# Kernel optimization log

Hardware: AMD Instinct MI355X
Metric: run time of the kernel (lower is better)

The kernel has to match this reference:

```python
import jax, jax.numpy as jnp
import numpy as np

EPS = 1e-6

def _ln(x, g, b):
    m = jnp.mean(x, -1, keepdims=True)
    v = jnp.mean((x - m) ** 2, -1, keepdims=True)
    return (x - m) * jax.lax.rsqrt(v + 1e-5) * g + b

def _mha(qin, kin, vin, wq, bq, wk, bk, wv, bv, wo, bo, nh=8):
    B, T, D = qin.shape
    S = kin.shape[1]
    dh = D // nh
    q = (qin @ wq + bq).reshape(B, T, nh, dh)
    k = (kin @ wk + bk).reshape(B, S, nh, dh)
    v = (vin @ wv + bv).reshape(B, S, nh, dh)
    a = jax.nn.softmax(jnp.einsum('bthd,bshd->bhts', q, k) / np.float32(np.sqrt(dh)), -1)
    o = jnp.einsum('bhts,bshd->bthd', a, v).reshape(B, T, D)
    return o @ wo + bo

def _sinu_pe(pos, num_feats=128, temperature=20.0):
    # pos: [..., 2] (x, y); returns [..., 2*num_feats] ordered (y-feats, x-feats)
    dim_t = temperature ** ((2 * (jnp.arange(num_feats) // 2)) / num_feats)
    e = pos[..., None] * (2 * np.pi) / dim_t  # [..., 2, F]
    e = jnp.stack([jnp.sin(e[..., 0::2]), jnp.cos(e[..., 1::2])], -1).reshape(e.shape)
    return jnp.concatenate([e[..., 1, :], e[..., 0, :]], -1)

def _spatial36(b1, b2, sizes):
    # b1, b2: [B, Q, 4]; sizes: [B, 2] = (h, w). UPT-style 18 feats + log -> 36.
    h = sizes[:, 0:1]; w = sizes[:, 1:2]
    c1x = (b1[..., 0] + b1[..., 2]) / 2; c1y = (b1[..., 1] + b1[..., 3]) / 2
    c2x = (b2[..., 0] + b2[..., 2]) / 2; c2y = (b2[..., 1] + b2[..., 3]) / 2
    w1 = b1[..., 2] - b1[..., 0]; h1 = b1[..., 3] - b1[..., 1]
    w2 = b2[..., 2] - b2[..., 0]; h2 = b2[..., 3] - b2[..., 1]
    a1 = w1 * h1; a2 = w2 * h2
    dx = jnp.abs(c2x - c1x) / (w1 + EPS)
    dy = jnp.abs(c2y - c1y) / (h1 + EPS)
    ix = jnp.clip(jnp.minimum(b1[..., 2], b2[..., 2]) - jnp.maximum(b1[..., 0], b2[..., 0]), 0)
    iy = jnp.clip(jnp.minimum(b1[..., 3], b2[..., 3]) - jnp.maximum(b1[..., 1], b2[..., 1]), 0)
    inter = ix * iy
    iou = inter / (a1 + a2 - inter + EPS)
    f = jnp.stack([c1x / w, c1y / h, c2x / w, c2y / h, w1 / w, h1 / h, w2 / w, h2 / h,
                   a1 / (h * w), a2 / (h * w), a2 / (a1 + EPS), w1 / (h1 + EPS), w2 / (h2 + EPS), iou,
                   (c2x > c1x) * dx, (c2x < c1x) * dx, (c2y > c1y) * dy, (c2y < c1y) * dy], -1)
    return jnp.concatenate([f, jnp.log(f + EPS)], -1)

def _forward(boxes, embeds, image_sizes, pose, line, sw1, sb1, sw2, sb2, sw3, sb3, bw, bb, pw, pb, lw, lb, enc_pe_w, enc_pe_b, enc_qkv_w, enc_qkv_b, enc_out_w, enc_out_b, enc_ff1_w, enc_ff1_b, enc_ff2_w, enc_ff2_b, enc_ln1_g, enc_ln1_b, enc_ln2_g, enc_ln2_b, dec_q_w, dec_q_b, dec_kv_w, dec_kv_b, dec_out_w, dec_out_b, dec_ff1_w, dec_ff1_b, dec_ff2_w, dec_ff2_b, dec_ln1_g, dec_ln1_b, dec_ln2_g, dec_ln2_b, fc1_w, fc1_b, fc2_w, fc2_b, mln1_g, mln1_b, mln2_g, mln2_b, m1_w, m1_b, m2_w, m2_b, labels, nh):
    B, N, _ = boxes.shape
    # static human-object pairing (x != y) & (x < nh)
    xg, yg = np.meshgrid(np.arange(N), np.arange(N), indexing='ij')
    keep = (xg != yg) & (xg < nh)
    xk = jnp.asarray(xg[keep]); yk = jnp.asarray(yg[keep])  # [P]
    # line features: adaptive-avg-pool(1,1) + 1x1 conv == spatial mean + linear
    line_feat = jnp.mean(line, axis=(2, 3)) @ lw + lb  # [B, 256]
    # spatial head on all N*N ordered pairs, then gather kept pairs
    xa = jnp.asarray(xg.reshape(-1)); ya = jnp.asarray(yg.reshape(-1))
    f36 = _spatial36(boxes[:, xa], boxes[:, ya], image_sizes)  # [B, N*N, 36]
    s = jax.nn.relu(f36 @ sw1 + sb1)
    s = jax.nn.relu(s @ sw2 + sb2)
    s = jax.nn.relu(s @ sw3 + sb3)
    spa = s.reshape(B, N, N, -1)[:, xk, yk]  # [B, P, R]
    # box sinusoidal positional encodings (cat of centre-PE and wh-PE)
    whwh = image_sizes[:, jnp.array([1, 0, 1, 0])][:, None]  # [B,1,4]
    bxn = boxes / whwh
    ctr = (bxn[..., :2] + bxn[..., 2:]) / 2
    whb = bxn[..., 2:] - bxn[..., :2]
    box_pe = jnp.concatenate([_sinu_pe(ctr), _sinu_pe(whb)], -1)  # [B, N, 512]
    # 2-layer transformer encoder over instance tokens (pos added to q,k)
    posx = box_pe @ enc_pe_w + enc_pe_b
    x = embeds
    for i in range(enc_qkv_w.shape[0]):
        wq, wk_, wv = jnp.split(enc_qkv_w[i], 3, axis=1)
        bq, bk_, bv = jnp.split(enc_qkv_b[i], 3)
        qk = x + posx
        att = _mha(qk, qk, x, wq, bq, wk_, bk_, wv, bv, enc_out_w[i], enc_out_b[i])
        x = _ln(x + att, enc_ln1_g[i], enc_ln1_b[i])
        ff = jax.nn.relu(x @ enc_ff1_w[i] + enc_ff1_b[i]) @ enc_ff2_w[i] + enc_ff2_b[i]
        x = _ln(x + ff, enc_ln2_g[i], enc_ln2_b[i])
    # pair gather + human/object positional embeds (box PE projected + line feature)
    pe_h = box_pe[:, xk] @ bw + bb + line_feat[:, None, :]
    pe_o = box_pe[:, yk] @ bw + bb + line_feat[:, None, :]
    h = x[:, xk]; o = x[:, yk]  # [B, P, 256]
    pose_ctx = pose @ pw + pb  # [B, M, 256]
    # HO refine decoder: cross-attention from pair tokens to pose tokens
    for l in range(dec_q_w.shape[0]):
        wk_, wv = jnp.split(dec_kv_w[l], 2, axis=1)
        bk_, bv = jnp.split(dec_kv_b[l], 2)
        def _layer(feat, pe):
            att = _mha(feat + pe, pose_ctx, pose_ctx, dec_q_w[l], dec_q_b[l], wk_, bk_, wv, bv, dec_out_w[l], dec_out_b[l])
            feat = _ln(feat + att, dec_ln1_g[l], dec_ln1_b[l])
            ff = jax.nn.relu(feat @ dec_ff1_w[l] + dec_ff1_b[l]) @ dec_ff2_w[l] + dec_ff2_b[l]
            return _ln(feat + ff, dec_ln2_g[l], dec_ln2_b[l])
        h = _layer(h, pe_h)
        o = _layer(o, pe_o)
    # multi-modal fusion
    ho = jnp.concatenate([h, o], -1)  # [B, P, 512]
    ho = _ln(ho @ fc1_w + fc1_b, mln1_g, mln1_b)
    sp = _ln(spa @ fc2_w + fc2_b, mln2_g, mln2_b)
    z = jax.nn.relu(jnp.concatenate([ho, sp], -1))
    z = jax.nn.relu(z @ m1_w + m1_b)
    z = jax.nn.relu(z @ m2_w + m2_b)
    return z  # [B, P, 256] HOI query features

def setup_inputs() -> dict:
    key = jax.random.key(0)
    ks = iter(jax.random.split(key, 80))
    B, N, NH, M, HH, WW = 16, 128, 32, 64, 8, 8
    W = 0.05
    def rn(shape, s=1.0):
        return jax.random.normal(next(ks), shape, dtype=jnp.float32) * s
    def ru(shape):
        return jax.random.uniform(next(ks), shape, dtype=jnp.float32)
    sizes = 800.0 + 480.0 * ru((B, 2))  # (h, w)
    wh = sizes[:, jnp.array([1, 0])]
    xy = ru((B, N, 2)) * wh[:, None] * 0.7
    bwh = ru((B, N, 2)) * wh[:, None] * 0.25 + 4.0
    boxes = jnp.concatenate([xy, xy + bwh], -1)
    labels = jnp.concatenate([jnp.zeros((B, NH), jnp.int32), jax.random.randint(next(ks), (B, N - NH), 1, 81, dtype=jnp.int32)], -1)
    return dict(
        boxes=boxes, embeds=rn((B, N, 256)), image_sizes=sizes, pose=rn((B, M, 768)), line=rn((B, 2048, HH, WW)),
        sw1=rn((36, 128), W), sb1=jnp.zeros((128,)), sw2=rn((128, 256), W), sb2=jnp.zeros((256,)), sw3=rn((256, 256), W), sb3=jnp.zeros((256,)),
        bw=rn((512, 256), W), bb=jnp.zeros((256,)), pw=rn((768, 256), W), pb=jnp.zeros((256,)), lw=rn((2048, 256), W), lb=jnp.zeros((256,)),
        enc_pe_w=rn((512, 256), W), enc_pe_b=jnp.zeros((256,)),
        enc_qkv_w=rn((2, 256, 768), W), enc_qkv_b=jnp.zeros((2, 768)), enc_out_w=rn((2, 256, 256), W), enc_out_b=jnp.zeros((2, 256)),
        enc_ff1_w=rn((2, 256, 1024), W), enc_ff1_b=jnp.zeros((2, 1024)), enc_ff2_w=rn((2, 1024, 256), W), enc_ff2_b=jnp.zeros((2, 256)),
        enc_ln1_g=jnp.ones((2, 256)), enc_ln1_b=jnp.zeros((2, 256)), enc_ln2_g=jnp.ones((2, 256)), enc_ln2_b=jnp.zeros((2, 256)),
        dec_q_w=rn((2, 256, 256), W), dec_q_b=jnp.zeros((2, 256)), dec_kv_w=rn((2, 256, 512), W), dec_kv_b=jnp.zeros((2, 512)),
        dec_out_w=rn((2, 256, 256), W), dec_out_b=jnp.zeros((2, 256)),
        dec_ff1_w=rn((2, 256, 1024), W), dec_ff1_b=jnp.zeros((2, 1024)), dec_ff2_w=rn((2, 1024, 256), W), dec_ff2_b=jnp.zeros((2, 256)),
        dec_ln1_g=jnp.ones((2, 256)), dec_ln1_b=jnp.zeros((2, 256)), dec_ln2_g=jnp.ones((2, 256)), dec_ln2_b=jnp.zeros((2, 256)),
        fc1_w=rn((512, 256), W), fc1_b=jnp.zeros((256,)), fc2_w=rn((256, 256), W), fc2_b=jnp.zeros((256,)),
        mln1_g=jnp.ones((256,)), mln1_b=jnp.zeros((256,)), mln2_g=jnp.ones((256,)), mln2_b=jnp.zeros((256,)),
        m1_w=rn((512, 384), W), m1_b=jnp.zeros((384,)), m2_w=rn((384, 256), W), m2_b=jnp.zeros((256,)),
        labels=labels, nh=NH)

def reference(boxes, embeds, image_sizes, pose, line, sw1, sb1, sw2, sb2, sw3, sb3, bw, bb, pw, pb, lw, lb, enc_pe_w, enc_pe_b, enc_qkv_w, enc_qkv_b, enc_out_w, enc_out_b, enc_ff1_w, enc_ff1_b, enc_ff2_w, enc_ff2_b, enc_ln1_g, enc_ln1_b, enc_ln2_g, enc_ln2_b, dec_q_w, dec_q_b, dec_kv_w, dec_kv_b, dec_out_w, dec_out_b, dec_ff1_w, dec_ff1_b, dec_ff2_w, dec_ff2_b, dec_ln1_g, dec_ln1_b, dec_ln2_g, dec_ln2_b, fc1_w, fc1_b, fc2_w, fc2_b, mln1_g, mln1_b, mln2_g, mln2_b, m1_w, m1_b, m2_w, m2_b, labels, nh):
    return _forward(boxes, embeds, image_sizes, pose, line, sw1, sb1, sw2, sb2, sw3, sb3, bw, bb, pw, pb, lw, lb, enc_pe_w, enc_pe_b, enc_qkv_w, enc_qkv_b, enc_out_w, enc_out_b, enc_ff1_w, enc_ff1_b, enc_ff2_w, enc_ff2_b, enc_ln1_g, enc_ln1_b, enc_ln2_g, enc_ln2_b, dec_q_w, dec_q_b, dec_kv_w, dec_kv_b, dec_out_w, dec_out_b, dec_ff1_w, dec_ff1_b, dec_ff2_w, dec_ff2_b, dec_ln1_g, dec_ln1_b, dec_ln2_g, dec_ln2_b, fc1_w, fc1_b, fc2_w, fc2_b, mln1_g, mln1_b, mln2_g, mln2_b, m1_w, m1_b, m2_w, m2_b, labels, nh)
```

## Files before the change

kernel.cpp:

```cpp
#include <hip/hip_runtime.h>
#include <stdint.h>

static constexpr int B      = 16;
static constexpr int N      = 128;
static constexpr int P      = 4064;
static constexpr int MPOSE  = 64;
static constexpr int64_t BN = (int64_t)B * N;
static constexpr int64_t BP = (int64_t)B * P;

#define TWO_PI 6.283185307179586f
#define QSCALE 0.17677669529663687f

typedef __attribute__((ext_vector_type(4))) float f32x4;
typedef __attribute__((ext_vector_type(8))) short bf16x8;
typedef __attribute__((ext_vector_type(8))) unsigned short u16x8;
typedef __attribute__((ext_vector_type(4))) unsigned short u16x4;

__device__ __forceinline__ unsigned short f2bf(float f) {
    union { float f; unsigned u; } v; v.f = f;
    unsigned r = (v.u + 0x7fffu + ((v.u >> 16) & 1u)) >> 16;
    return (unsigned short)r;
}
__device__ __forceinline__ float bf2f(unsigned short u) {
    union { unsigned u; float f; } v; v.u = (unsigned)u << 16;
    return v.f;
}
__device__ __forceinline__ void pair_xy(int p, int& x, int& y) {
    x = p / 127;
    int r = p - x * 127;
    y = (r < x) ? r : r + 1;
}

struct WDesc { const float* src; int64_t dstOff; int K, Nn, Kpad, blockStart; };
struct WTable { WDesc d[29]; int nDesc; };

__global__ __launch_bounds__(256) void wprep_all_k(WTable t, unsigned short* __restrict__ wt)
{
    __shared__ float s[32][33];
    int bid = blockIdx.x;
    int di = 0;
    for (int i = 1; i < t.nDesc; ++i) if (t.d[i].blockStart <= bid) di = i;
    const WDesc& d = t.d[di];
    int lbid = bid - d.blockStart;
    int kTiles = d.Kpad >> 5;
    int k0 = (lbid % kTiles) * 32, n0 = (lbid / kTiles) * 32;
    int tx = threadIdx.x & 31, ty = threadIdx.x >> 5;
#pragma unroll
    for (int i = 0; i < 4; ++i) {
        int k = k0 + ty + i * 8;
        s[ty + i * 8][tx] = (k < d.K) ? d.src[(int64_t)k * d.Nn + n0 + tx] : 0.f;
    }
    __syncthreads();
    unsigned short* dst = wt + d.dstOff;
#pragma unroll
    for (int i = 0; i < 4; ++i) {
        int n = n0 + ty + i * 8;
        dst[(int64_t)n * d.Kpad + k0 + tx] = f2bf(s[tx][ty + i * 8]);
    }
}

template <bool RELU_OUT, bool RELU_A>
__global__ __launch_bounds__(256) void bgemm_k(
    const float* __restrict__ A, const float* __restrict__ A2, int lda,
    const unsigned short* __restrict__ Bt, int ldk,
    const float* __restrict__ bias,
    float* __restrict__ C, int ldc,
    int K, int kSteps)
{
    __shared__ unsigned short As[128][40];
    __shared__ unsigned short Bs[128][40];
    const int tid  = threadIdx.x;
    const int lane = tid & 63;
    const int wave = tid >> 6;
    const int wr = wave >> 1, wc = wave & 1;
    const int row0 = blockIdx.y * 128, col0 = blockIdx.x * 128;
    const int l15 = lane & 15, l4 = lane >> 4;
    const int sr = tid >> 1;
    const int sh = (tid & 1) * 16;

    f32x4 acc[4][4] = {};

    for (int ks = 0; ks < kSteps; ++ks) {
        const int k0 = ks * 32;
        {
            const int64_t off = (int64_t)(row0 + sr) * lda + k0 + sh;
            const float* ap = A + off;
            float v[16];
#pragma unroll
            for (int i = 0; i < 4; ++i) {
                float4 tv = ((const float4*)ap)[i];
                v[i*4+0] = tv.x; v[i*4+1] = tv.y; v[i*4+2] = tv.z; v[i*4+3] = tv.w;
            }
            if (A2) {
                const float* ap2 = A2 + off;
#pragma unroll
                for (int i = 0; i < 4; ++i) {
                    float4 tv = ((const float4*)ap2)[i];
                    v[i*4+0] += tv.x; v[i*4+1] += tv.y; v[i*4+2] += tv.z; v[i*4+3] += tv.w;
                }
            }
            if (RELU_A) {
#pragma unroll
                for (int j = 0; j < 16; ++j) v[j] = fmaxf(v[j], 0.f);
            }
            u16x8 p0, p1;
#pragma unroll
            for (int j = 0; j < 8; ++j) { p0[j] = f2bf(v[j]); p1[j] = f2bf(v[8 + j]); }
            *(u16x8*)&As[sr][sh]     = p0;
            *(u16x8*)&As[sr][sh + 8] = p1;
        }
        {
            const unsigned short* bp = Bt + (int64_t)(col0 + sr) * ldk + k0 + sh;
            u16x8 q0 = *(const u16x8*)bp;
            u16x8 q1 = *(const u16x8*)(bp + 8);
            *(u16x8*)&Bs[sr][sh]     = q0;
            *(u16x8*)&Bs[sr][sh + 8] = q1;
        }
        __syncthreads();
        bf16x8 af[4], bfr[4];
#pragma unroll
        for (int f = 0; f < 4; ++f) {
            af[f]  = *(const bf16x8*)&As[wr * 64 + f * 16 + l15][l4 * 8];
            bfr[f] = *(const bf16x8*)&Bs[wc * 64 + f * 16 + l15][l4 * 8];
        }
#pragma unroll
        for (int i = 0; i < 4; ++i)
#pragma unroll
            for (int j = 0; j < 4; ++j)
                acc[i][j] = __builtin_amdgcn_mfma_f32_16x16x32_bf16(af[i], bfr[j], acc[i][j], 0, 0, 0);
        __syncthreads();
    }
#pragma unroll
    for (int i = 0; i < 4; ++i) {
        int rb = row0 + wr * 64 + i * 16 + l4 * 4;
#pragma unroll
        for (int j = 0; j < 4; ++j) {
            int c = col0 + wc * 64 + j * 16 + l15;
            float bv = bias ? bias[c] : 0.f;
#pragma unroll
            for (int e = 0; e < 4; ++e) {
                float vv = acc[i][j][e] + bv;
                if (RELU_OUT) vv = fmaxf(vv, 0.f);
                C[(int64_t)(rb + e) * ldc + c] = vv;
            }
        }
    }
}

static void bgemm(hipStream_t st,
                  const float* A, const float* A2, int lda,
                  const unsigned short* Bt, int ldk, const float* bias,
                  float* C, int ldc, int M, int Ncols, int K,
                  bool reluOut, bool reluA)
{
    int kSteps = K / 32;
    dim3 g(Ncols / 128, M / 128), b(256);
    if (!reluOut && !reluA)      bgemm_k<false,false><<<g,b,0,st>>>(A,A2,lda,Bt,ldk,bias,C,ldc,K,kSteps);
    else if (reluOut && !reluA)  bgemm_k<true,false><<<g,b,0,st>>>(A,A2,lda,Bt,ldk,bias,C,ldc,K,kSteps);
    else if (!reluOut && reluA)  bgemm_k<false,true><<<g,b,0,st>>>(A,A2,lda,Bt,ldk,bias,C,ldc,K,kSteps);
    else                         bgemm_k<true,true><<<g,b,0,st>>>(A,A2,lda,Bt,ldk,bias,C,ldc,K,kSteps);
}

template <bool RELU_A, bool RELU2, bool OUT_BF16>
__global__ __launch_bounds__(256) void fgemm_k(
    const unsigned short* __restrict__ A, int lda,
    const unsigned short* __restrict__ W1, int ldk1, const float* __restrict__ b1,
    const unsigned short* __restrict__ W2, int ldk2, const float* __restrict__ b2,
    void* __restrict__ Cv, int ldc,
    int ksteps1, int n1tiles)
{
    __shared__ unsigned short As[128][40];
    __shared__ unsigned short Bs[128][40];
    __shared__ unsigned short D1s[128][136];
    const int tid  = threadIdx.x;
    const int lane = tid & 63;
    const int wave = tid >> 6;
    const int wr = wave >> 1, wc = wave & 1;
    const int row0 = blockIdx.x * 128;
    const int l15 = lane & 15, l4 = lane >> 4;
    const int sr = tid >> 1;
    const int sh = (tid & 1) * 16;

    f32x4 acc2[2][4][4] = {};

    for (int j = 0; j < n1tiles; ++j) {
        f32x4 acc1[4][4] = {};
        for (int ks = 0; ks < ksteps1; ++ks) {
            const int k0 = ks * 32;
            {
                const unsigned short* ap = A + (int64_t)(row0 + sr) * lda + k0 + sh;
                u16x8 q0 = *(const u16x8*)ap;
                u16x8 q1 = *(const u16x8*)(ap + 8);
                if (RELU_A) {
#pragma unroll
                    for (int q = 0; q < 8; ++q) {
                        q0[q] = (q0[q] & 0x8000u) ? 0 : q0[q];
                        q1[q] = (q1[q] & 0x8000u) ? 0 : q1[q];
                    }
                }
                *(u16x8*)&As[sr][sh]     = q0;
                *(u16x8*)&As[sr][sh + 8] = q1;
            }
            {
                const unsigned short* bp = W1 + (int64_t)(j * 128 + sr) * ldk1 + k0 + sh;
                *(u16x8*)&Bs[sr][sh]     = *(const u16x8*)bp;
                *(u16x8*)&Bs[sr][sh + 8] = *(const u16x8*)(bp + 8);
            }
            __syncthreads();
            bf16x8 af[4], bfr[4];
#pragma unroll
            for (int f = 0; f < 4; ++f) {
                af[f]  = *(const bf16x8*)&As[wr * 64 + f * 16 + l15][l4 * 8];
                bfr[f] = *(const bf16x8*)&Bs[wc * 64 + f * 16 + l15][l4 * 8];
            }
#pragma unroll
            for (int i = 0; i < 4; ++i)
#pragma unroll
                for (int jj = 0; jj < 4; ++jj)
                    acc1[i][jj] = __builtin_amdgcn_mfma_f32_16x16x32_bf16(af[i], bfr[jj], acc1[i][jj], 0, 0, 0);
            __syncthreads();
        }
#pragma unroll
        for (int i = 0; i < 4; ++i) {
            int rb = wr * 64 + i * 16 + l4 * 4;
#pragma unroll
            for (int jj = 0; jj < 4; ++jj) {
                int c = wc * 64 + jj * 16 + l15;
                float bv = b1[j * 128 + c];
#pragma unroll
                for (int e = 0; e < 4; ++e) {
                    float vv = fmaxf(acc1[i][jj][e] + bv, 0.f);
                    D1s[rb + e][c] = f2bf(vv);
                }
            }
        }
        __syncthreads();
#pragma unroll
        for (int n = 0; n < 2; ++n) {
            for (int kk = 0; kk < 4; ++kk) {
                {
                    const unsigned short* bp = W2 + (int64_t)(n * 128 + sr) * ldk2 + j * 128 + kk * 32 + sh;
                    *(u16x8*)&Bs[sr][sh]     = *(const u16x8*)bp;
                    *(u16x8*)&Bs[sr][sh + 8] = *(const u16x8*)(bp + 8);
                }
                __syncthreads();
                bf16x8 af[4], bfr[4];
#pragma unroll
                for (int f = 0; f < 4; ++f) {
                    af[f]  = *(const bf16x8*)&D1s[wr * 64 + f * 16 + l15][kk * 32 + l4 * 8];
                    bfr[f] = *(const bf16x8*)&Bs[wc * 64 + f * 16 + l15][l4 * 8];
                }
#pragma unroll
                for (int i = 0; i < 4; ++i)
#pragma unroll
                    for (int jj = 0; jj < 4; ++jj)
                        acc2[n][i][jj] = __builtin_amdgcn_mfma_f32_16x16x32_bf16(af[i], bfr[jj], acc2[n][i][jj], 0, 0, 0);
                __syncthreads();
            }
        }
    }
#pragma unroll
    for (int n = 0; n < 2; ++n)
#pragma unroll
    for (int i = 0; i < 4; ++i) {
        int rb = row0 + wr * 64 + i * 16 + l4 * 4;
#pragma unroll
        for (int jj = 0; jj < 4; ++jj) {
            int c = n * 128 + wc * 64 + jj * 16 + l15;
            float bv = b2[c];
#pragma unroll
            for (int e = 0; e < 4; ++e) {
                float vv = acc2[n][i][jj][e] + bv;
                if (RELU2) vv = fmaxf(vv, 0.f);
                int64_t off = (int64_t)(rb + e) * ldc + c;
                if (OUT_BF16) ((unsigned short*)Cv)[off] = f2bf(vv);
                else          ((float*)Cv)[off] = vv;
            }
        }
    }
}

__global__ __launch_bounds__(256) void ln_k(
    float* __restrict__ out, const float* __restrict__ x, const float* __restrict__ res,
    const float* __restrict__ g, const float* __restrict__ be, int rows)
{
    int wave = threadIdx.x >> 6, lane = threadIdx.x & 63;
    int row = blockIdx.x * 4 + wave;
    if (row >= rows) return;
    int64_t base = (int64_t)row * 256 + lane * 4;
    float4 v = *(const float4*)(x + base);
    if (res) {
        float4 r = *(const float4*)(res + base);
        v.x += r.x; v.y += r.y; v.z += r.z; v.w += r.w;
    }
    float s  = v.x + v.y + v.z + v.w;
    float sq = v.x*v.x + v.y*v.y + v.z*v.z + v.w*v.w;
#pragma unroll
    for (int off = 1; off < 64; off <<= 1) {
        s  += __shfl_xor(s, off);
        sq += __shfl_xor(sq, off);
    }
    float m = s * (1.f/256.f);
    float var = sq * (1.f/256.f) - m * m;
    float inv = rsqrtf(var + 1e-5f);
    int c = lane * 4;
    float4 gg = *(const float4*)(g + c);
    float4 bb = *(const float4*)(be + c);
    float4 o;
    o.x = (v.x - m) * inv * gg.x + bb.x;
    o.y = (v.y - m) * inv * gg.y + bb.y;
    o.z = (v.z - m) * inv * gg.z + bb.z;
    o.w = (v.w - m) * inv * gg.w + bb.w;
    *(float4*)(out + base) = o;
}

__global__ __launch_bounds__(256) void lnh_k(
    unsigned short* __restrict__ outp, int ldo,
    const unsigned short* __restrict__ x, int ldx,
    const float* __restrict__ g, const float* __restrict__ be, int rows)
{
    int wave = threadIdx.x >> 6, lane = threadIdx.x & 63;
    int row = blockIdx.x * 4 + wave;
    if (row >= rows) return;
    u16x4 u = *(const u16x4*)(x + (int64_t)row * ldx + lane * 4);
    float4 v;
    v.x = bf2f(u[0]); v.y = bf2f(u[1]); v.z = bf2f(u[2]); v.w = bf2f(u[3]);
    float s  = v.x + v.y + v.z + v.w;
    float sq = v.x*v.x + v.y*v.y + v.z*v.z + v.w*v.w;
#pragma unroll
    for (int off = 1; off < 64; off <<= 1) {
        s  += __shfl_xor(s, off);
        sq += __shfl_xor(sq, off);
    }
    float m = s * (1.f/256.f);
    float var = sq * (1.f/256.f) - m * m;
    float inv = rsqrtf(var + 1e-5f);
    int c = lane * 4;
    float4 gg = *(const float4*)(g + c);
    float4 bb = *(const float4*)(be + c);
    u16x4 o;
    o[0] = f2bf((v.x - m) * inv * gg.x + bb.x);
    o[1] = f2bf((v.y - m) * inv * gg.y + bb.y);
    o[2] = f2bf((v.z - m) * inv * gg.z + bb.z);
    o[3] = f2bf((v.w - m) * inv * gg.w + bb.w);
    *(u16x4*)(outp + (int64_t)row * ldo + c) = o;
}

__global__ __launch_bounds__(256) void pairln_k(
    const float* __restrict__ UV,
    const float* __restrict__ fb,
    const float* __restrict__ g, const float* __restrict__ be,
    unsigned short* __restrict__ outp, int ldo, int chunk0, int rows)
{
    int wave = threadIdx.x >> 6, lane = threadIdx.x & 63;
    int li = blockIdx.x * 4 + wave;
    if (li >= rows) return;
    int gp = chunk0 + li;
    int b = gp / P, p = gp - b * P;
    int xi, yi; pair_xy(p, xi, yi);
    int c = lane * 4;
    float4 u  = *(const float4*)(UV + ((int64_t)(b * 128 + xi)) * 512 + c);
    float4 vv = *(const float4*)(UV + ((int64_t)(b * 128 + yi)) * 512 + 256 + c);
    float4 fbv = *(const float4*)(fb + c);
    float4 v;
    v.x = u.x + vv.x + fbv.x; v.y = u.y + vv.y + fbv.y;
    v.z = u.z + vv.z + fbv.z; v.w = u.w + vv.w + fbv.w;
    float s  = v.x + v.y + v.z + v.w;
    float sq = v.x*v.x + v.y*v.y + v.z*v.z + v.w*v.w;
#pragma unroll
    for (int off = 1; off < 64; off <<= 1) {
        s  += __shfl_xor(s, off);
        sq += __shfl_xor(sq, off);
    }
    float m = s * (1.f/256.f);
    float var = sq * (1.f/256.f) - m * m;
    float inv = rsqrtf(var + 1e-5f);
    float4 gg = *(const float4*)(g + c);
    float4 bb = *(const float4*)(be + c);
    u16x4 o;
    o[0] = f2bf((v.x - m) * inv * gg.x + bb.x);
    o[1] = f2bf((v.y - m) * inv * gg.y + bb.y);
    o[2] = f2bf((v.z - m) * inv * gg.z + bb.z);
    o[3] = f2bf((v.w - m) * inv * gg.w + bb.w);
    *(u16x4*)(outp + (int64_t)li * ldo + c) = o;
}

__global__ __launch_bounds__(256) void line_mean_k(const float* __restrict__ line, float* __restrict__ lm)
{
    int wave = threadIdx.x >> 6, lane = threadIdx.x & 63;
    int bc = blockIdx.x * 4 + wave;
    float v = line[(int64_t)bc * 64 + lane];
#pragma unroll
    for (int off = 1; off < 64; off <<= 1) v += __shfl_xor(v, off);
    if (lane == 0) lm[bc] = v * (1.f/64.f);
}

__global__ __launch_bounds__(256) void line_proj_k(
    const float* __restrict__ lm, const float* __restrict__ lw,
    const float* __restrict__ lb, float* __restrict__ lf)
{
    __shared__ float red[8][32];
    int b = blockIdx.y, jg = blockIdx.x;
    int jj = threadIdx.x & 31, cc = threadIdx.x >> 5;
    int j = jg * 32 + jj;
    const float* lmb = lm + (int64_t)b * 2048 + cc * 256;
    const float* lwp = lw + (int64_t)(cc * 256) * 256 + j;
    float acc = 0.f;
#pragma unroll 4
    for (int k = 0; k < 256; ++k) acc += lmb[k] * lwp[(int64_t)k * 256];
    red[cc][jj] = acc;
    __syncthreads();
    if (cc == 0) {
        float s = lb[j];
#pragma unroll
        for (int i = 0; i < 8; ++i) s += red[i][jj];
        lf[b * 256 + j] = s;
    }
}

__global__ __launch_bounds__(256) void add_lf_k(float* __restrict__ bpw, const float* __restrict__ lf)
{
    int r = blockIdx.x, c = threadIdx.x;
    bpw[(int64_t)r * 256 + c] += lf[(r >> 7) * 256 + c];
}

__global__ __launch_bounds__(512) void boxpe_k(
    const float* __restrict__ boxes, const float* __restrict__ sizes, float* __restrict__ boxpe)
{
    int row = blockIdx.x;
    int b = row >> 7;
    int i = threadIdx.x;
    const float* bx = boxes + (int64_t)row * 4;
    float h = sizes[b * 2 + 0], w = sizes[b * 2 + 1];
    float x0 = bx[0] / w, y0 = bx[1] / h, x1 = bx[2] / w, y1 = bx[3] / h;
    int seg = i >> 7, j = i & 127, k = j >> 1;
    float val;
    switch (seg) {
        case 0: val = (y0 + y1) * 0.5f; break;
        case 1: val = (x0 + x1) * 0.5f; break;
        case 2: val = (y1 - y0); break;
        default: val = (x1 - x0); break;
    }
    float dimt = exp2f((float)k * (4.321928094887362f / 64.f));
    float arg = val * TWO_PI / dimt;
    boxpe[(int64_t)row * 512 + i] = (j & 1) ? cosf(arg) : sinf(arg);
}

__global__ __launch_bounds__(256) void f36_k(
    const float* __restrict__ boxes, const float* __restrict__ sizes,
    unsigned short* __restrict__ f36, int chunk0, int cnt)
{
    int li = blockIdx.x * 256 + threadIdx.x;
    if (li >= cnt) return;
    int gp = chunk0 + li;
    int b = gp / P, p = gp - b * P;
    int xi, yi; pair_xy(p, xi, yi);
    const float* b1 = boxes + ((int64_t)b * N + xi) * 4;
    const float* b2 = boxes + ((int64_t)b * N + yi) * 4;
    float h = sizes[b * 2 + 0], w = sizes[b * 2 + 1];
    float c1x = (b1[0] + b1[2]) * 0.5f, c1y = (b1[1] + b1[3]) * 0.5f;
    float c2x = (b2[0] + b2[2]) * 0.5f, c2y = (b2[1] + b2[3]) * 0.5f;
    float w1 = b1[2] - b1[0], h1 = b1[3] - b1[1];
    float w2 = b2[2] - b2[0], h2 = b2[3] - b2[1];
    float a1 = w1 * h1, a2 = w2 * h2;
    float dx = fabsf(c2x - c1x) / (w1 + 1e-6f);
    float dy = fabsf(c2y - c1y) / (h1 + 1e-6f);
    float ix = fmaxf(fminf(b1[2], b2[2]) - fmaxf(b1[0], b2[0]), 0.f);
    float iy = fmaxf(fminf(b1[3], b2[3]) - fmaxf(b1[1], b2[1]), 0.f);
    float inter = ix * iy;
    float iou = inter / (a1 + a2 - inter + 1e-6f);
    float f[18];
    f[0] = c1x / w;  f[1] = c1y / h;  f[2] = c2x / w;  f[3] = c2y / h;
    f[4] = w1 / w;   f[5] = h1 / h;   f[6] = w2 / w;   f[7] = h2 / h;
    f[8] = a1 / (h * w); f[9] = a2 / (h * w); f[10] = a2 / (a1 + 1e-6f);
    f[11] = w1 / (h1 + 1e-6f); f[12] = w2 / (h2 + 1e-6f); f[13] = iou;
    f[14] = (c2x > c1x) ? dx : 0.f;  f[15] = (c2x < c1x) ? dx : 0.f;
    f[16] = (c2y > c1y) ? dy : 0.f;  f[17] = (c2y < c1y) ? dy : 0.f;
    unsigned short* o = f36 + (int64_t)li * 64;
#pragma unroll
    for (int i = 0; i < 18; ++i) {
        o[i]      = f2bf(f[i]);
        o[18 + i] = f2bf(logf(f[i] + 1e-6f));
    }
#pragma unroll
    for (int i = 36; i < 64; ++i) o[i] = 0;
}

__global__ __launch_bounds__(128) void enc_attn_k(
    const float* __restrict__ qk, const float* __restrict__ v, float* __restrict__ outp)
{
    int b = blockIdx.x >> 3, hd = blockIdx.x & 7;
    __shared__ float kl[128][32];
    __shared__ float vl[128][32];
    int tid = threadIdx.x;
    for (int i = tid; i < 128 * 32; i += 128) {
        int s = i >> 5, j = i & 31;
        kl[s][j] = qk[((int64_t)(b * 128 + s)) * 512 + 256 + hd * 32 + j];
        vl[s][j] = v[((int64_t)(b * 128 + s)) * 256 + hd * 32 + j];
    }
    __syncthreads();
    int t = tid;
    const float* qp = qk + ((int64_t)(b * 128 + t)) * 512 + hd * 32;
    float qr[32];
#pragma unroll
    for (int j = 0; j < 32; ++j) qr[j] = qp[j] * QSCALE;
    float m = -1e30f, l = 0.f;
    for (int s = 0; s < 128; ++s) {
        float d = 0.f;
#pragma unroll
        for (int j = 0; j < 32; ++j) d += qr[j] * kl[s][j];
        float mn = fmaxf(m, d);
        l = l * __expf(m - mn) + __expf(d - mn);
        m = mn;
    }
    float acc[32] = {};
    for (int s = 0; s < 128; ++s) {
        float d = 0.f;
#pragma unroll
        for (int j = 0; j < 32; ++j) d += qr[j] * kl[s][j];
        float wgt = __expf(d - m);
#pragma unroll
        for (int j = 0; j < 32; ++j) acc[j] += wgt * vl[s][j];
    }
    float linv = 1.f / l;
    float* op = outp + ((int64_t)(b * 128 + t)) * 256 + hd * 32;
#pragma unroll
    for (int j = 0; j < 32; ++j) op[j] = acc[j] * linv;
}

__global__ __launch_bounds__(256) void dec_attn_k(
    const float* __restrict__ q, const float* __restrict__ kv,
    float* __restrict__ outp, int rows, int rpb)
{
    int hd = blockIdx.y;
    int r0 = blockIdx.x * 256;
    __shared__ float kl[2][64][32];
    __shared__ float vl[2][64][32];
    int tid = threadIdx.x;
    int b0 = r0 / rpb;
    int b1 = (r0 + 255) / rpb;
    if (b1 >= B) b1 = B - 1;
    for (int i = tid; i < 64 * 32; i += 256) {
        int s = i >> 5, j = i & 31;
        int64_t off0 = ((int64_t)(b0 * MPOSE + s)) * 512 + hd * 32 + j;
        int64_t off1 = ((int64_t)(b1 * MPOSE + s)) * 512 + hd * 32 + j;
        kl[0][s][j] = kv[off0];
        vl[0][s][j] = kv[off0 + 256];
        kl[1][s][j] = kv[off1];
        vl[1][s][j] = kv[off1 + 256];
    }
    __syncthreads();
    int r = r0 + tid;
    if (r >= rows) return;
    int which = (r / rpb == b0) ? 0 : 1;
    int64_t qoff = (int64_t)r * 256 + hd * 32;
    float qr[32];
#pragma unroll
    for (int j = 0; j < 32; ++j) qr[j] = q[qoff + j] * QSCALE;
    float m = -1e30f, l = 0.f;
    for (int s = 0; s < 64; ++s) {
        float d = 0.f;
#pragma unroll
        for (int j = 0; j < 32; ++j) d += qr[j] * kl[which][s][j];
        float mn = fmaxf(m, d);
        l = l * __expf(m - mn) + __expf(d - mn);
        m = mn;
    }
    float acc[32] = {};
    for (int s = 0; s < 64; ++s) {
        float d = 0.f;
#pragma unroll
        for (int j = 0; j < 32; ++j) d += qr[j] * kl[which][s][j];
        float wgt = __expf(d - m);
#pragma unroll
        for (int j = 0; j < 32; ++j) acc[j] += wgt * vl[which][s][j];
    }
    float linv = 1.f / l;
#pragma unroll
    for (int j = 0; j < 32; ++j) outp[qoff + j] = acc[j] * linv;
}

static constexpr int64_t WT_QKV  = 0;
static constexpr int64_t WT_EOUT = WT_QKV  + 2*196608;
static constexpr int64_t WT_EFF1 = WT_EOUT + 2*65536;
static constexpr int64_t WT_EFF2 = WT_EFF1 + 2*262144;
static constexpr int64_t WT_DQ   = WT_EFF2 + 2*262144;
static constexpr int64_t WT_DKV  = WT_DQ   + 2*65536;
static constexpr int64_t WT_DOUT = WT_DKV  + 2*131072;
static constexpr int64_t WT_DFF1 = WT_DOUT + 2*65536;
static constexpr int64_t WT_DFF2 = WT_DFF1 + 2*262144;
static constexpr int64_t WT_SW1  = WT_DFF2 + 2*262144;
static constexpr int64_t WT_SW2  = WT_SW1 + 8192;
static constexpr int64_t WT_SW3  = WT_SW2 + 32768;
static constexpr int64_t WT_BW   = WT_SW3 + 65536;
static constexpr int64_t WT_PW   = WT_BW  + 131072;
static constexpr int64_t WT_EPE  = WT_PW  + 196608;
static constexpr int64_t WT_FC1  = WT_EPE + 131072;
static constexpr int64_t WT_FC2  = WT_FC1 + 131072;
static constexpr int64_t WT_M1   = WT_FC2 + 65536;
static constexpr int64_t WT_M2   = WT_M1  + 196608;
static constexpr int64_t WT_TOTAL = WT_M2 + 98304;

extern "C" void kernel_launch(void* const* d_in, const int* in_sizes, int n_in,
                              void* d_out, int out_size, void* d_ws, size_t ws_size,
                              hipStream_t stream)
{
    (void)in_sizes; (void)n_in; (void)out_size;
    const float* boxes     = (const float*)d_in[0];
    const float* embeds    = (const float*)d_in[1];
    const float* sizes     = (const float*)d_in[2];
    const float* pose      = (const float*)d_in[3];
    const float* line      = (const float*)d_in[4];
    const float* sw1 = (const float*)d_in[5];  const float* sb1 = (const float*)d_in[6];
    const float* sw2 = (const float*)d_in[7];  const float* sb2 = (const float*)d_in[8];
    const float* sw3 = (const float*)d_in[9];  const float* sb3 = (const float*)d_in[10];
    const float* bw  = (const float*)d_in[11]; const float* bb  = (const float*)d_in[12];
    const float* pw  = (const float*)d_in[13]; const float* pb  = (const float*)d_in[14];
    const float* lw  = (const float*)d_in[15]; const float* lb  = (const float*)d_in[16];
    const float* enc_pe_w  = (const float*)d_in[17]; const float* enc_pe_b = (const float*)d_in[18];
    const float* enc_qkv_w = (const float*)d_in[19]; const float* enc_qkv_b = (const float*)d_in[20];
    const float* enc_out_w = (const float*)d_in[21]; const float* enc_out_b = (const float*)d_in[22];
    const float* enc_ff1_w = (const float*)d_in[23]; const float* enc_ff1_b = (const float*)d_in[24];
    const float* enc_ff2_w = (const float*)d_in[25]; const float* enc_ff2_b = (const float*)d_in[26];
    const float* enc_ln1_g = (const float*)d_in[27]; const float* enc_ln1_b = (const float*)d_in[28];
    const float* enc_ln2_g = (const float*)d_in[29]; const float* enc_ln2_b = (const float*)d_in[30];
    const float* dec_q_w   = (const float*)d_in[31]; const float* dec_q_b  = (const float*)d_in[32];
    const float* dec_kv_w  = (const float*)d_in[33]; const float* dec_kv_b = (const float*)d_in[34];
    const float* dec_out_w = (const float*)d_in[35]; const float* dec_out_b = (const float*)d_in[36];
    const float* dec_ff1_w = (const float*)d_in[37]; const float* dec_ff1_b = (const float*)d_in[38];
    const float* dec_ff2_w = (const float*)d_in[39]; const float* dec_ff2_b = (const float*)d_in[40];
    const float* dec_ln1_g = (const float*)d_in[41]; const float* dec_ln1_b = (const float*)d_in[42];
    const float* dec_ln2_g = (const float*)d_in[43]; const float* dec_ln2_b = (const float*)d_in[44];
    const float* fc1_w = (const float*)d_in[45]; const float* fc1_b = (const float*)d_in[46];
    const float* fc2_w = (const float*)d_in[47]; const float* fc2_b = (const float*)d_in[48];
    const float* mln1_g = (const float*)d_in[49]; const float* mln1_b = (const float*)d_in[50];
    const float* mln2_g = (const float*)d_in[51]; const float* mln2_b = (const float*)d_in[52];
    const float* m1_w = (const float*)d_in[53]; const float* m1_b = (const float*)d_in[54];
    const float* m2_w = (const float*)d_in[55]; const float* m2_b = (const float*)d_in[56];
    float* out = (float*)d_out;

    float* base = (float*)d_ws;
    int64_t wsf = (int64_t)(ws_size / sizeof(float));
    float* x_   = base;
    float* bpw_ = x_   + 524288;
    float* lf   = bpw_ + 524288;
    float* kv0  = lf   + 4096;
    unsigned short* wt = (unsigned short*)(kv0 + 2 * 524288);
    float* arena = (float*)(wt + WT_TOTAL);
    const int64_t LIVE_F = arena - base;
    int64_t arena_f = wsf - LIVE_F;
    if (arena_f < 0) arena_f = 0;

    float* posx  = arena;
    float* boxpe = posx  + 524288;
    float* e_qk  = boxpe + 1048576;
    float* e_v   = e_qk  + 1048576;
    float* e_t   = e_v   + 524288;
    float* e_ff  = e_t   + 524288;
    float* pctx  = e_ff  + 2097152;
    float* lm    = pctx  + 262144;

    int64_t rc = ((arena_f * 2) / 1088) & ~127LL;
    if (rc > BP) rc = BP;
    if (rc < 128) rc = 128;

    {
        WTable T;
        int nd = 0, bs = 0;
        auto add = [&](const float* src, int64_t dstOff, int K, int Nn, int Kpad) {
            T.d[nd] = { src, dstOff, K, Nn, Kpad, bs };
            bs += (Kpad / 32) * (Nn / 32);
            ++nd;
        };
        for (int i = 0; i < 2; ++i) {
            add(enc_qkv_w + (int64_t)i*196608, WT_QKV  + i*196608, 256, 768, 256);
            add(enc_out_w + (int64_t)i*65536,  WT_EOUT + i*65536,  256, 256, 256);
            add(enc_ff1_w + (int64_t)i*262144, WT_EFF1 + i*262144, 256, 1024, 256);
            add(enc_ff2_w + (int64_t)i*262144, WT_EFF2 + i*262144, 1024, 256, 1024);
            add(dec_q_w   + (int64_t)i*65536,  WT_DQ   + i*65536,  256, 256, 256);
            add(dec_kv_w  + (int64_t)i*131072, WT_DKV  + i*131072, 256, 512, 256);
            add(dec_out_w + (int64_t)i*65536,  WT_DOUT + i*65536,  256, 256, 256);
            add(dec_ff1_w + (int64_t)i*262144, WT_DFF1 + i*262144, 256, 1024, 256);
            add(dec_ff2_w + (int64_t)i*262144, WT_DFF2 + i*262144, 1024, 256, 1024);
        }
        add(sw1, WT_SW1, 36, 128, 64);
        add(sw2, WT_SW2, 128, 256, 128);
        add(sw3, WT_SW3, 256, 256, 256);
        add(bw,  WT_BW,  512, 256, 512);
        add(pw,  WT_PW,  768, 256, 768);
        add(enc_pe_w, WT_EPE, 512, 256, 512);
        add(fc1_w,             WT_FC1,         256, 256, 256);
        add(fc1_w + 256 * 256, WT_FC1 + 65536, 256, 256, 256);
        add(fc2_w, WT_FC2, 256, 256, 256);
        add(m1_w, WT_M1, 512, 384, 512);
        add(m2_w, WT_M2, 384, 256, 384);
        T.nDesc = nd;
        wprep_all_k<<<bs, 256, 0, stream>>>(T, wt);
    }

    line_mean_k<<<8192, 256, 0, stream>>>(line, lm);
    line_proj_k<<<dim3(8, B), 256, 0, stream>>>(lm, lw, lb, lf);
    boxpe_k<<<(int)BN, 512, 0, stream>>>(boxes, sizes, boxpe);
    bgemm(stream, boxpe, nullptr, 512, wt + WT_EPE, 512, enc_pe_b, posx, 256, (int)BN, 256, 512, false, false);
    bgemm(stream, boxpe, nullptr, 512, wt + WT_BW,  512, bb,       bpw_, 256, (int)BN, 256, 512, false, false);
    bgemm(stream, pose,  nullptr, 768, wt + WT_PW,  768, pb,       pctx, 256, B*MPOSE, 256, 768, false, false);
    for (int l = 0; l < 2; ++l)
        bgemm(stream, pctx, nullptr, 256, wt + WT_DKV + l*131072, 256, dec_kv_b + (int64_t)l*512,
              kv0 + (int64_t)l*524288, 512, B*MPOSE, 512, 256, false, false);

    hipMemcpyAsync(x_, embeds, BN * 256 * sizeof(float), hipMemcpyDeviceToDevice, stream);
    for (int i = 0; i < 2; ++i) {
        const unsigned short* Wq = wt + WT_QKV + (int64_t)i * 196608;
        const float* bqkv = enc_qkv_b + (int64_t)i * 768;
        bgemm(stream, x_, posx, 256, Wq, 256, bqkv, e_qk, 512, (int)BN, 512, 256, false, false);
        bgemm(stream, x_, nullptr, 256, Wq + 131072, 256, bqkv + 512, e_v, 256, (int)BN, 256, 256, false, false);
        enc_attn_k<<<B * 8, 128, 0, stream>>>(e_qk, e_v, e_t);
        bgemm(stream, e_t, nullptr, 256, wt + WT_EOUT + (int64_t)i*65536, 256, enc_out_b + i * 256,
              e_v, 256, (int)BN, 256, 256, false, false);
        ln_k<<<(int)(BN / 4), 256, 0, stream>>>(x_, x_, e_v, enc_ln1_g + i * 256, enc_ln1_b + i * 256, (int)BN);
        bgemm(stream, x_, nullptr, 256, wt + WT_EFF1 + (int64_t)i*262144, 256, enc_ff1_b + i * 1024,
              e_ff, 1024, (int)BN, 1024, 256, true, false);
        bgemm(stream, e_ff, nullptr, 1024, wt + WT_EFF2 + (int64_t)i*262144, 1024, enc_ff2_b + i * 256,
              e_t, 256, (int)BN, 256, 1024, false, false);
        ln_k<<<(int)(BN / 4), 256, 0, stream>>>(x_, x_, e_t, enc_ln2_g + i * 256, enc_ln2_b + i * 256, (int)BN);
    }

    add_lf_k<<<(int)BN, 256, 0, stream>>>(bpw_, lf);
    for (int l = 0; l < 2; ++l) {
        bgemm(stream, x_, bpw_, 256, wt + WT_DQ + (int64_t)l*65536, 256, dec_q_b + l * 256,
              e_v, 256, (int)BN, 256, 256, false, false);
        dec_attn_k<<<dim3((int)(BN / 256), 8), 256, 0, stream>>>(e_v, kv0 + (int64_t)l*524288, e_t, (int)BN, N);
        bgemm(stream, e_t, nullptr, 256, wt + WT_DOUT + (int64_t)l*65536, 256, dec_out_b + l * 256,
              e_v, 256, (int)BN, 256, 256, false, false);
        ln_k<<<(int)(BN / 4), 256, 0, stream>>>(x_, x_, e_v, dec_ln1_g + l * 256, dec_ln1_b + l * 256, (int)BN);
        bgemm(stream, x_, nullptr, 256, wt + WT_DFF1 + (int64_t)l*262144, 256, dec_ff1_b + l * 1024,
              e_ff, 1024, (int)BN, 1024, 256, true, false);
        bgemm(stream, e_ff, nullptr, 1024, wt + WT_DFF2 + (int64_t)l*262144, 1024, dec_ff2_b + l * 256,
              e_t, 256, (int)BN, 256, 1024, false, false);
        ln_k<<<(int)(BN / 4), 256, 0, stream>>>(x_, x_, e_t, dec_ln2_g + l * 256, dec_ln2_b + l * 256, (int)BN);
    }
    float* UV = kv0;
    bgemm(stream, x_, nullptr, 256, wt + WT_FC1, 256, nullptr, UV, 512, (int)BN, 512, 256, false, false);

    for (int64_t c0 = 0; c0 < BP; c0 += rc) {
        int rows = (int)((BP - c0 < rc) ? (BP - c0) : rc);
        unsigned short* t1  = (unsigned short*)arena;
        unsigned short* t3  = t1  + (int64_t)rc * 64;
        unsigned short* tsp = t3  + (int64_t)rc * 256;
        unsigned short* zb  = tsp + (int64_t)rc * 256;

        f36_k<<<(rows + 255) / 256, 256, 0, stream>>>(boxes, sizes, t1, (int)c0, rows);
        fgemm_k<false,true,true><<<rows / 128, 256, 0, stream>>>(
            t1, 64, wt + WT_SW1, 64, sb1, wt + WT_SW2, 128, sb2, t3, 256, 2, 1);
        fgemm_k<false,false,true><<<rows / 128, 256, 0, stream>>>(
            t3, 256, wt + WT_SW3, 256, sb3, wt + WT_FC2, 256, fc2_b, tsp, 256, 8, 2);
        lnh_k<<<rows / 4, 256, 0, stream>>>(zb + 256, 512, tsp, 256, mln2_g, mln2_b, rows);
        pairln_k<<<rows / 4, 256, 0, stream>>>(UV, fc1_b, mln1_g, mln1_b, zb, 512, (int)c0, rows);
        fgemm_k<true,true,false><<<rows / 128, 256, 0, stream>>>(
            zb, 512, wt + WT_M1, 512, m1_b, wt + WT_M2, 384, m2_b, out + c0 * 256, 256, 16, 3);
    }
}
```

Baseline: 889.6 us.

## Fuse GEMM epilogues with LayerNorm, merge QKV, and restructure pair MLP kernels

Several changes land together. The encoder/decoder out-projection and FF2 GEMMs now apply residual add and LayerNorm in a new full-row GEMM kernel, which removes the separate ln_k passes. Q/K/V become one GEMM, with the positional QK term precomputed and added in the epilogue. The line-feature add is folded into the box projection epilogue. In the pair path, box-feature computation is fused into the first MLP kernel and fc2 is fused with its LayerNorm. The final fused m1/m2 kernel is split into two tiled GEMMs with a bf16 intermediate, which trades extra memory traffic for more parallelism and no recomputation.

After: 906.6 us. About the same (+1.9%).

```diff
diff --git a/kernel.cpp b/kernel.cpp
--- a/kernel.cpp
+++ b/kernel.cpp
@@ -59,13 +59,15 @@
     }
 }
 
-template <bool RELU_OUT, bool RELU_A>
+template <bool RELU_OUT>
 __global__ __launch_bounds__(256) void bgemm_k(
     const float* __restrict__ A, const float* __restrict__ A2, int lda,
     const unsigned short* __restrict__ Bt, int ldk,
     const float* __restrict__ bias,
+    const float* __restrict__ Cadd, int addLd,
+    const float* __restrict__ lfp,
     float* __restrict__ C, int ldc,
-    int K, int kSteps)
+    int kSteps)
 {
     __shared__ unsigned short As[128][40];
     __shared__ unsigned short Bs[128][40];
@@ -99,10 +101,6 @@
                     v[i*4+0] += tv.x; v[i*4+1] += tv.y; v[i*4+2] += tv.z; v[i*4+3] += tv.w;
                 }
             }
-            if (RELU_A) {
-#pragma unroll
-                for (int j = 0; j < 16; ++j) v[j] = fmaxf(v[j], 0.f);
-            }
             u16x8 p0, p1;
 #pragma unroll
             for (int j = 0; j < 8; ++j) { p0[j] = f2bf(v[j]); p1[j] = f2bf(v[8 + j]); }
@@ -111,10 +109,8 @@
         }
         {
             const unsigned short* bp = Bt + (int64_t)(col0 + sr) * ldk + k0 + sh;
-            u16x8 q0 = *(const u16x8*)bp;
-            u16x8 q1 = *(const u16x8*)(bp + 8);
-            *(u16x8*)&Bs[sr][sh]     = q0;
-            *(u16x8*)&Bs[sr][sh + 8] = q1;
+            *(u16x8*)&Bs[sr][sh]     = *(const u16x8*)bp;
+            *(u16x8*)&Bs[sr][sh + 8] = *(const u16x8*)(bp + 8);
         }
         __syncthreads();
         bf16x8 af[4], bfr[4];
@@ -139,9 +135,12 @@
             float bv = bias ? bias[c] : 0.f;
 #pragma unroll
             for (int e = 0; e < 4; ++e) {
+                int r = rb + e;
                 float vv = acc[i][j][e] + bv;
+                if (Cadd && c < addLd) vv += Cadd[(int64_t)r * addLd + c];
+                if (lfp) vv += lfp[(r >> 7) * 256 + c];
                 if (RELU_OUT) vv = fmaxf(vv, 0.f);
-                C[(int64_t)(rb + e) * ldc + c] = vv;
+                C[(int64_t)r * ldc + c] = vv;
             }
         }
     }
@@ -150,26 +149,204 @@
 static void bgemm(hipStream_t st,
                   const float* A, const float* A2, int lda,
                   const unsigned short* Bt, int ldk, const float* bias,
-                  float* C, int ldc, int M, int Ncols, int K,
-                  bool reluOut, bool reluA)
-{
-    int kSteps = K / 32;
+                  const float* Cadd, int addLd, const float* lfp,
+                  float* C, int ldc, int M, int Ncols, int K, bool reluOut)
+{
     dim3 g(Ncols / 128, M / 128), b(256);
-    if (!reluOut && !reluA)      bgemm_k<false,false><<<g,b,0,st>>>(A,A2,lda,Bt,ldk,bias,C,ldc,K,kSteps);
-    else if (reluOut && !reluA)  bgemm_k<true,false><<<g,b,0,st>>>(A,A2,lda,Bt,ldk,bias,C,ldc,K,kSteps);
-    else if (!reluOut && reluA)  bgemm_k<false,true><<<g,b,0,st>>>(A,A2,lda,Bt,ldk,bias,C,ldc,K,kSteps);
-    else                         bgemm_k<true,true><<<g,b,0,st>>>(A,A2,lda,Bt,ldk,bias,C,ldc,K,kSteps);
-}
-
-template <bool RELU_A, bool RELU2, bool OUT_BF16>
-__global__ __launch_bounds__(256) void fgemm_k(
+    if (reluOut) bgemm_k<true><<<g,b,0,st>>>(A,A2,lda,Bt,ldk,bias,Cadd,addLd,lfp,C,ldc,K/32);
+    else         bgemm_k<false><<<g,b,0,st>>>(A,A2,lda,Bt,ldk,bias,Cadd,addLd,lfp,C,ldc,K/32);
+}
+
+__global__ __launch_bounds__(256) void tgemm_k(
+    const float* __restrict__ A, int lda,
+    const unsigned short* __restrict__ Bt, int ldk,
+    const float* __restrict__ bias,
+    const float* __restrict__ res,
+    const float* __restrict__ g, const float* __restrict__ be,
+    float* __restrict__ C, int kSteps)
+{
+    __shared__ unsigned short As[64][40];
+    __shared__ unsigned short Bs[256][40];
+    __shared__ float partS[64][4], partQ[64][4];
+    __shared__ float statM[64], statI[64];
+    const int tid = threadIdx.x;
+    const int lane = tid & 63, w = tid >> 6;
+    const int l15 = lane & 15, l4 = lane >> 4;
+    const int row0 = blockIdx.x * 64;
+    const int sra = tid >> 2, sha = (tid & 3) * 8;
+
+    f32x4 acc[4][4] = {};
+    for (int ks = 0; ks < kSteps; ++ks) {
+        int k0 = ks * 32;
+        {
+            const float* ap = A + (int64_t)(row0 + sra) * lda + k0 + sha;
+            float4 t0 = ((const float4*)ap)[0];
+            float4 t1 = ((const float4*)ap)[1];
+            u16x8 p;
+            p[0]=f2bf(t0.x); p[1]=f2bf(t0.y); p[2]=f2bf(t0.z); p[3]=f2bf(t0.w);
+            p[4]=f2bf(t1.x); p[5]=f2bf(t1.y); p[6]=f2bf(t1.z); p[7]=f2bf(t1.w);
+            *(u16x8*)&As[sra][sha] = p;
+        }
+        {
+            const unsigned short* bp = Bt + (int64_t)tid * ldk + k0;
+#pragma unroll
+            for (int q = 0; q < 4; ++q)
+                *(u16x8*)&Bs[tid][q * 8] = *(const u16x8*)(bp + q * 8);
+        }
+        __syncthreads();
+        bf16x8 af[4], bfr[4];
+#pragma unroll
+        for (int f = 0; f < 4; ++f) {
+            af[f]  = *(const bf16x8*)&As[f * 16 + l15][l4 * 8];
+            bfr[f] = *(const bf16x8*)&Bs[w * 64 + f * 16 + l15][l4 * 8];
+        }
+#pragma unroll
+        for (int i = 0; i < 4; ++i)
+#pragma unroll
+            for (int j = 0; j < 4; ++j)
+                acc[i][j] = __builtin_amdgcn_mfma_f32_16x16x32_bf16(af[i], bfr[j], acc[i][j], 0, 0, 0);
+        __syncthreads();
+    }
+    float ps[4][4] = {}, pq[4][4] = {};
+#pragma unroll
+    for (int i = 0; i < 4; ++i)
+#pragma unroll
+    for (int j = 0; j < 4; ++j) {
+        int c = w * 64 + j * 16 + l15;
+#pragma unroll
+        for (int e = 0; e < 4; ++e) {
+            int r = i * 16 + l4 * 4 + e;
+            float v = acc[i][j][e] + bias[c] + res[(int64_t)(row0 + r) * 256 + c];
+            acc[i][j][e] = v;
+            ps[i][e] += v;
+            pq[i][e] += v * v;
+        }
+    }
+#pragma unroll
+    for (int i = 0; i < 4; ++i)
+#pragma unroll
+    for (int e = 0; e < 4; ++e) {
+#pragma unroll
+        for (int m = 1; m < 16; m <<= 1) {
+            ps[i][e] += __shfl_xor(ps[i][e], m);
+            pq[i][e] += __shfl_xor(pq[i][e], m);
+        }
+    }
+    if (l15 == 0) {
+#pragma unroll
+        for (int i = 0; i < 4; ++i)
+#pragma unroll
+        for (int e = 0; e < 4; ++e) {
+            int r = i * 16 + l4 * 4 + e;
+            partS[r][w] = ps[i][e];
+            partQ[r][w] = pq[i][e];
+        }
+    }
+    __syncthreads();
+    if (tid < 64) {
+        float s = partS[tid][0] + partS[tid][1] + partS[tid][2] + partS[tid][3];
+        float q = partQ[tid][0] + partQ[tid][1] + partQ[tid][2] + partQ[tid][3];
+        float m = s * (1.f/256.f);
+        float var = q * (1.f/256.f) - m * m;
+        statM[tid] = m;
+        statI[tid] = rsqrtf(var + 1e-5f);
+    }
+    __syncthreads();
+#pragma unroll
+    for (int i = 0; i < 4; ++i)
+#pragma unroll
+    for (int j = 0; j < 4; ++j) {
+        int c = w * 64 + j * 16 + l15;
+#pragma unroll
+        for (int e = 0; e < 4; ++e) {
+            int r = i * 16 + l4 * 4 + e;
+            C[(int64_t)(row0 + r) * 256 + c] = (acc[i][j][e] - statM[r]) * statI[r] * g[c] + be[c];
+        }
+    }
+}
+
+template <bool RELU_OUT, bool RELU_A, bool OUT_BF16>
+__global__ __launch_bounds__(256) void hgemm_k(
     const unsigned short* __restrict__ A, int lda,
-    const unsigned short* __restrict__ W1, int ldk1, const float* __restrict__ b1,
-    const unsigned short* __restrict__ W2, int ldk2, const float* __restrict__ b2,
+    const unsigned short* __restrict__ Bt, int ldk,
+    const float* __restrict__ bias,
     void* __restrict__ Cv, int ldc,
-    int ksteps1, int n1tiles)
+    int kSteps)
 {
     __shared__ unsigned short As[128][40];
+    __shared__ unsigned short Bs[128][40];
+    const int tid  = threadIdx.x;
+    const int lane = tid & 63;
+    const int wave = tid >> 6;
+    const int wr = wave >> 1, wc = wave & 1;
+    const int row0 = blockIdx.y * 128, col0 = blockIdx.x * 128;
+    const int l15 = lane & 15, l4 = lane >> 4;
+    const int sr = tid >> 1;
+    const int sh = (tid & 1) * 16;
+
+    f32x4 acc[4][4] = {};
+
+    for (int ks = 0; ks < kSteps; ++ks) {
+        const int k0 = ks * 32;
+        {
+            const unsigned short* ap = A + (int64_t)(row0 + sr) * lda + k0 + sh;
+            u16x8 q0 = *(const u16x8*)ap;
+            u16x8 q1 = *(const u16x8*)(ap + 8);
+            if (RELU_A) {
+#pragma unroll
+                for (int q = 0; q < 8; ++q) {
+                    q0[q] = (q0[q] & 0x8000u) ? 0 : q0[q];
+                    q1[q] = (q1[q] & 0x8000u) ? 0 : q1[q];
+                }
+            }
+            *(u16x8*)&As[sr][sh]     = q0;
+            *(u16x8*)&As[sr][sh + 8] = q1;
+        }
+        {
+            const unsigned short* bp = Bt + (int64_t)(col0 + sr) * ldk + k0 + sh;
+            *(u16x8*)&Bs[sr][sh]     = *(const u16x8*)bp;
+            *(u16x8*)&Bs[sr][sh + 8] = *(const u16x8*)(bp + 8);
+        }
+        __syncthreads();
+        bf16x8 af[4], bfr[4];
+#pragma unroll
+        for (int f = 0; f < 4; ++f) {
+            af[f]  = *(const bf16x8*)&As[wr * 64 + f * 16 + l15][l4 * 8];
+            bfr[f] = *(const bf16x8*)&Bs[wc * 64 + f * 16 + l15][l4 * 8];
+        }
+#pragma unroll
+        for (int i = 0; i < 4; ++i)
+#pragma unroll
+            for (int j = 0; j < 4; ++j)
+                acc[i][j] = __builtin_amdgcn_mfma_f32_16x16x32_bf16(af[i], bfr[j], acc[i][j], 0, 0, 0);
+        __syncthreads();
+    }
+#pragma unroll
+    for (int i = 0; i < 4; ++i) {
+        int rb = row0 + wr * 64 + i * 16 + l4 * 4;
+#pragma unroll
+        for (int j = 0; j < 4; ++j) {
+            int c = col0 + wc * 64 + j * 16 + l15;
+            float bv = bias ? bias[c] : 0.f;
+#pragma unroll
+            for (int e = 0; e < 4; ++e) {
+                int64_t off = (int64_t)(rb + e) * ldc + c;
+                float vv = acc[i][j][e] + bv;
+                if (RELU_OUT) vv = fmaxf(vv, 0.f);
+                if (OUT_BF16) ((unsigned short*)Cv)[off] = f2bf(vv);
+                else          ((float*)Cv)[off] = vv;
+            }
+        }
+    }
+}
+
+__global__ __launch_bounds__(256) void spa_k(
+    const float* __restrict__ boxes, const float* __restrict__ sizes,
+    const unsigned short* __restrict__ W1, const float* __restrict__ b1,
+    const unsigned short* __restrict__ W2, const float* __restrict__ b2,
+    unsigned short* __restrict__ t3out, int chunk0)
+{
+    __shared__ unsigned short F[128][72];
     __shared__ unsigned short Bs[128][40];
     __shared__ unsigned short D1s[128][136];
     const int tid  = threadIdx.x;
@@ -181,28 +358,150 @@
     const int sr = tid >> 1;
     const int sh = (tid & 1) * 16;
 
+    if (tid < 128) {
+        int gp = chunk0 + row0 + tid;
+        int b = gp / P, p = gp - b * P;
+        int xi, yi; pair_xy(p, xi, yi);
+        const float* b1x = boxes + ((int64_t)b * N + xi) * 4;
+        const float* b2x = boxes + ((int64_t)b * N + yi) * 4;
+        float h = sizes[b * 2 + 0], w = sizes[b * 2 + 1];
+        float c1x = (b1x[0] + b1x[2]) * 0.5f, c1y = (b1x[1] + b1x[3]) * 0.5f;
+        float c2x = (b2x[0] + b2x[2]) * 0.5f, c2y = (b2x[1] + b2x[3]) * 0.5f;
+        float w1 = b1x[2] - b1x[0], h1 = b1x[3] - b1x[1];
+        float w2 = b2x[2] - b2x[0], h2 = b2x[3] - b2x[1];
+        float a1 = w1 * h1, a2 = w2 * h2;
+        float dx = fabsf(c2x - c1x) / (w1 + 1e-6f);
+        float dy = fabsf(c2y - c1y) / (h1 + 1e-6f);
+        float ix = fmaxf(fminf(b1x[2], b2x[2]) - fmaxf(b1x[0], b2x[0]), 0.f);
+        float iy = fmaxf(fminf(b1x[3], b2x[3]) - fmaxf(b1x[1], b2x[1]), 0.f);
+        float inter = ix * iy;
+        float iou = inter / (a1 + a2 - inter + 1e-6f);
+        float f[18];
+        f[0] = c1x / w;  f[1] = c1y / h;  f[2] = c2x / w;  f[3] = c2y / h;
+        f[4] = w1 / w;   f[5] = h1 / h;   f[6] = w2 / w;   f[7] = h2 / h;
+        f[8] = a1 / (h * w); f[9] = a2 / (h * w); f[10] = a2 / (a1 + 1e-6f);
+        f[11] = w1 / (h1 + 1e-6f); f[12] = w2 / (h2 + 1e-6f); f[13] = iou;
+        f[14] = (c2x > c1x) ? dx : 0.f;  f[15] = (c2x < c1x) ? dx : 0.f;
+        f[16] = (c2y > c1y) ? dy : 0.f;  f[17] = (c2y < c1y) ? dy : 0.f;
+#pragma unroll
+        for (int i = 0; i < 18; ++i) {
+            F[tid][i]      = f2bf(f[i]);
+            F[tid][18 + i] = f2bf(logf(f[i] + 1e-6f));
+        }
+#pragma unroll
+        for (int i = 36; i < 64; ++i) F[tid][i] = 0;
+    }
+    __syncthreads();
+
+    f32x4 acc1[4][4] = {};
+    for (int ks = 0; ks < 2; ++ks) {
+        const int k0 = ks * 32;
+        {
+            const unsigned short* bp = W1 + (int64_t)sr * 64 + k0 + sh;
+            *(u16x8*)&Bs[sr][sh]     = *(const u16x8*)bp;
+            *(u16x8*)&Bs[sr][sh + 8] = *(const u16x8*)(bp + 8);
+        }
+        __syncthreads();
+        bf16x8 af[4], bfr[4];
+#pragma unroll
+        for (int f = 0; f < 4; ++f) {
+            af[f]  = *(const bf16x8*)&F[wr * 64 + f * 16 + l15][k0 + l4 * 8];
+            bfr[f] = *(const bf16x8*)&Bs[wc * 64 + f * 16 + l15][l4 * 8];
+        }
+#pragma unroll
+        for (int i = 0; i < 4; ++i)
+#pragma unroll
+            for (int j = 0; j < 4; ++j)
+                acc1[i][j] = __builtin_amdgcn_mfma_f32_16x16x32_bf16(af[i], bfr[j], acc1[i][j], 0, 0, 0);
+        __syncthreads();
+    }
+#pragma unroll
+    for (int i = 0; i < 4; ++i) {
+        int rb = wr * 64 + i * 16 + l4 * 4;
+#pragma unroll
+        for (int j = 0; j < 4; ++j) {
+            int c = wc * 64 + j * 16 + l15;
+            float bv = b1[c];
+#pragma unroll
+            for (int e = 0; e < 4; ++e)
+                D1s[rb + e][c] = f2bf(fmaxf(acc1[i][j][e] + bv, 0.f));
+        }
+    }
+    __syncthreads();
+
     f32x4 acc2[2][4][4] = {};
-
-    for (int j = 0; j < n1tiles; ++j) {
+#pragma unroll
+    for (int n = 0; n < 2; ++n) {
+        for (int kk = 0; kk < 4; ++kk) {
+            {
+                const unsigned short* bp = W2 + (int64_t)(n * 128 + sr) * 128 + kk * 32 + sh;
+                *(u16x8*)&Bs[sr][sh]     = *(const u16x8*)bp;
+                *(u16x8*)&Bs[sr][sh + 8] = *(const u16x8*)(bp + 8);
+            }
+            __syncthreads();
+            bf16x8 af[4], bfr[4];
+#pragma unroll
+            for (int f = 0; f < 4; ++f) {
+                af[f]  = *(const bf16x8*)&D1s[wr * 64 + f * 16 + l15][kk * 32 + l4 * 8];
+                bfr[f] = *(const bf16x8*)&Bs[wc * 64 + f * 16 + l15][l4 * 8];
+            }
+#pragma unroll
+            for (int i = 0; i < 4; ++i)
+#pragma unroll
+                for (int j = 0; j < 4; ++j)
+                    acc2[n][i][j] = __builtin_amdgcn_mfma_f32_16x16x32_bf16(af[i], bfr[j], acc2[n][i][j], 0, 0, 0);
+            __syncthreads();
+        }
+    }
+#pragma unroll
+    for (int n = 0; n < 2; ++n)
+#pragma unroll
+    for (int i = 0; i < 4; ++i) {
+        int rb = row0 + wr * 64 + i * 16 + l4 * 4;
+#pragma unroll
+        for (int j = 0; j < 4; ++j) {
+            int c = n * 128 + wc * 64 + j * 16 + l15;
+            float bv = b2[c];
+#pragma unroll
+            for (int e = 0; e < 4; ++e)
+                t3out[(int64_t)(rb + e) * 256 + c] = f2bf(fmaxf(acc2[n][i][j][e] + bv, 0.f));
+        }
+    }
+}
+
+__global__ __launch_bounds__(256) void sw3fc2ln_k(
+    const unsigned short* __restrict__ A,
+    const unsigned short* __restrict__ W1, const float* __restrict__ b1,
+    const unsigned short* __restrict__ W2, const float* __restrict__ b2,
+    const float* __restrict__ g, const float* __restrict__ be,
+    unsigned short* __restrict__ outp, int ldo)
+{
+    __shared__ unsigned short As[128][40];
+    __shared__ unsigned short Bs[128][40];
+    __shared__ unsigned short D1s[128][136];
+    __shared__ float partS[128][2], partQ[128][2];
+    __shared__ float statM[128], statI[128];
+    const int tid  = threadIdx.x;
+    const int lane = tid & 63;
+    const int wave = tid >> 6;
+    const int wr = wave >> 1, wc = wave & 1;
+    const int row0 = blockIdx.x * 128;
+    const int l15 = lane & 15, l4 = lane >> 4;
+    const int sr = tid >> 1;
+    const int sh = (tid & 1) * 16;
+
+    f32x4 acc2[2][4][4] = {};
+    for (int j = 0; j < 2; ++j) {
         f32x4 acc1[4][4] = {};
-        for (int ks = 0; ks < ksteps1; ++ks) {
+        for (int ks = 0; ks < 8; ++ks) {
             const int k0 = ks * 32;
             {
-                const unsigned short* ap = A + (int64_t)(row0 + sr) * lda + k0 + sh;
-                u16x8 q0 = *(const u16x8*)ap;
-                u16x8 q1 = *(const u16x8*)(ap + 8);
-                if (RELU_A) {
-#pragma unroll
-                    for (int q = 0; q < 8; ++q) {
-                        q0[q] = (q0[q] & 0x8000u) ? 0 : q0[q];
-                        q1[q] = (q1[q] & 0x8000u) ? 0 : q1[q];
-                    }
-                }
-                *(u16x8*)&As[sr][sh]     = q0;
-                *(u16x8*)&As[sr][sh + 8] = q1;
+                const unsigned short* ap = A + (int64_t)(row0 + sr) * 256 + k0 + sh;
+                *(u16x8*)&As[sr][sh]     = *(const u16x8*)ap;
+                *(u16x8*)&As[sr][sh + 8] = *(const u16x8*)(ap + 8);
             }
             {
-                const unsigned short* bp = W1 + (int64_t)(j * 128 + sr) * ldk1 + k0 + sh;
+                const unsigned short* bp = W1 + (int64_t)(j * 128 + sr) * 256 + k0 + sh;
                 *(u16x8*)&Bs[sr][sh]     = *(const u16x8*)bp;
                 *(u16x8*)&Bs[sr][sh + 8] = *(const u16x8*)(bp + 8);
             }
@@ -228,10 +527,8 @@
                 int c = wc * 64 + jj * 16 + l15;
                 float bv = b1[j * 128 + c];
 #pragma unroll
-                for (int e = 0; e < 4; ++e) {
-                    float vv = fmaxf(acc1[i][jj][e] + bv, 0.f);
-                    D1s[rb + e][c] = f2bf(vv);
-                }
+                for (int e = 0; e < 4; ++e)
+                    D1s[rb + e][c] = f2bf(fmaxf(acc1[i][jj][e] + bv, 0.f));
             }
         }
         __syncthreads();
@@ -239,7 +536,7 @@
         for (int n = 0; n < 2; ++n) {
             for (int kk = 0; kk < 4; ++kk) {
                 {
-                    const unsigned short* bp = W2 + (int64_t)(n * 128 + sr) * ldk2 + j * 128 + kk * 32 + sh;
+                    const unsigned short* bp = W2 + (int64_t)(n * 128 + sr) * 256 + j * 128 + kk * 32 + sh;
                     *(u16x8*)&Bs[sr][sh]     = *(const u16x8*)bp;
                     *(u16x8*)&Bs[sr][sh + 8] = *(const u16x8*)(bp + 8);
                 }
@@ -259,96 +556,70 @@
             }
         }
     }
+    float ps[4][4] = {}, pq[4][4] = {};
 #pragma unroll
     for (int n = 0; n < 2; ++n)
 #pragma unroll
-    for (int i = 0; i < 4; ++i) {
-        int rb = row0 + wr * 64 + i * 16 + l4 * 4;
-#pragma unroll
-        for (int jj = 0; jj < 4; ++jj) {
-            int c = n * 128 + wc * 64 + jj * 16 + l15;
-            float bv = b2[c];
-#pragma unroll
-            for (int e = 0; e < 4; ++e) {
-                float vv = acc2[n][i][jj][e] + bv;
-                if (RELU2) vv = fmaxf(vv, 0.f);
-                int64_t off = (int64_t)(rb + e) * ldc + c;
-                if (OUT_BF16) ((unsigned short*)Cv)[off] = f2bf(vv);
-                else          ((float*)Cv)[off] = vv;
-            }
-        }
-    }
-}
-
-__global__ __launch_bounds__(256) void ln_k(
-    float* __restrict__ out, const float* __restrict__ x, const float* __restrict__ res,
-    const float* __restrict__ g, const float* __restrict__ be, int rows)
-{
-    int wave = threadIdx.x >> 6, lane = threadIdx.x & 63;
-    int row = blockIdx.x * 4 + wave;
-    if (row >= rows) return;
-    int64_t base = (int64_t)row * 256 + lane * 4;
-    float4 v = *(const float4*)(x + base);
-    if (res) {
-        float4 r = *(const float4*)(res + base);
-        v.x += r.x; v.y += r.y; v.z += r.z; v.w += r.w;
-    }
-    float s  = v.x + v.y + v.z + v.w;
-    float sq = v.x*v.x + v.y*v.y + v.z*v.z + v.w*v.w;
-#pragma unroll
-    for (int off = 1; off < 64; off <<= 1) {
-        s  += __shfl_xor(s, off);
-        sq += __shfl_xor(sq, off);
-    }
-    float m = s * (1.f/256.f);
-    float var = sq * (1.f/256.f) - m * m;
-    float inv = rsqrtf(var + 1e-5f);
-    int c = lane * 4;
-    float4 gg = *(const float4*)(g + c);
-    float4 bb = *(const float4*)(be + c);
-    float4 o;
-    o.x = (v.x - m) * inv * gg.x + bb.x;
-    o.y = (v.y - m) * inv * gg.y + bb.y;
-    o.z = (v.z - m) * inv * gg.z + bb.z;
-    o.w = (v.w - m) * inv * gg.w + bb.w;
-    *(float4*)(out + base) = o;
-}
-
-__global__ __launch_bounds__(256) void lnh_k(
-    unsigned short* __restrict__ outp, int ldo,
-    const unsigned short* __restrict__ x, int ldx,
-    const float* __restrict__ g, const float* __restrict__ be, int rows)
-{
-    int wave = threadIdx.x >> 6, lane = threadIdx.x & 63;
-    int row = blockIdx.x * 4 + wave;
-    if (row >= rows) return;
-    u16x4 u = *(const u16x4*)(x + (int64_t)row * ldx + lane * 4);
-    float4 v;
-    v.x = bf2f(u[0]); v.y = bf2f(u[1]); v.z = bf2f(u[2]); v.w = bf2f(u[3]);
-    float s  = v.x + v.y + v.z + v.w;
-    float sq = v.x*v.x + v.y*v.y + v.z*v.z + v.w*v.w;
-#pragma unroll
-    for (int off = 1; off < 64; off <<= 1) {
-        s  += __shfl_xor(s, off);
-        sq += __shfl_xor(sq, off);
-    }
-    float m = s * (1.f/256.f);
-    float var = sq * (1.f/256.f) - m * m;
-    float inv = rsqrtf(var + 1e-5f);
-    int c = lane * 4;
-    float4 gg = *(const float4*)(g + c);
-    float4 bb = *(const float4*)(be + c);
-    u16x4 o;
-    o[0] = f2bf((v.x - m) * inv * gg.x + bb.x);
-    o[1] = f2bf((v.y - m) * inv * gg.y + bb.y);
-    o[2] = f2bf((v.z - m) * inv * gg.z + bb.z);
-    o[3] = f2bf((v.w - m) * inv * gg.w + bb.w);
-    *(u16x4*)(outp + (int64_t)row * ldo + c) = o;
+    for (int i = 0; i < 4; ++i)
+#pragma unroll
+    for (int jj = 0; jj < 4; ++jj) {
+        int c = n * 128 + wc * 64 + jj * 16 + l15;
+#pragma unroll
+        for (int e = 0; e < 4; ++e) {
+            float v = acc2[n][i][jj][e] + b2[c];
+            acc2[n][i][jj][e] = v;
+            ps[i][e] += v;
+            pq[i][e] += v * v;
+        }
+    }
+#pragma unroll
+    for (int i = 0; i < 4; ++i)
+#pragma unroll
+    for (int e = 0; e < 4; ++e) {
+#pragma unroll
+        for (int m = 1; m < 16; m <<= 1) {
+            ps[i][e] += __shfl_xor(ps[i][e], m);
+            pq[i][e] += __shfl_xor(pq[i][e], m);
+        }
+    }
+    if (l15 == 0) {
+#pragma unroll
+        for (int i = 0; i < 4; ++i)
+#pragma unroll
+        for (int e = 0; e < 4; ++e) {
+            int r = wr * 64 + i * 16 + l4 * 4 + e;
+            partS[r][wc] = ps[i][e];
+            partQ[r][wc] = pq[i][e];
+        }
+    }
+    __syncthreads();
+    if (tid < 128) {
+        float s = partS[tid][0] + partS[tid][1];
+        float q = partQ[tid][0] + partQ[tid][1];
+        float m = s * (1.f/256.f);
+        float var = q * (1.f/256.f) - m * m;
+        statM[tid] = m;
+        statI[tid] = rsqrtf(var + 1e-5f);
+    }
+    __syncthreads();
+#pragma unroll
+    for (int n = 0; n < 2; ++n)
+#pragma unroll
+    for (int i = 0; i < 4; ++i)
+#pragma unroll
+    for (int jj = 0; jj < 4; ++jj) {
+        int c = n * 128 + wc * 64 + jj * 16 + l15;
+#pragma unroll
+        for (int e = 0; e < 4; ++e) {
+            int r = wr * 64 + i * 16 + l4 * 4 + e;
+            float o = (acc2[n][i][jj][e] - statM[r]) * statI[r] * g[c] + be[c];
+            outp[(int64_t)(row0 + r) * ldo + c] = f2bf(o);
+        }
+    }
 }
 
 __global__ __launch_bounds__(256) void pairln_k(
-    const float* __restrict__ UV,
-    const float* __restrict__ fb,
+    const float* __restrict__ UV, const float* __restrict__ fb,
     const float* __restrict__ g, const float* __restrict__ be,
     unsigned short* __restrict__ outp, int ldo, int chunk0, int rows)
 {
@@ -418,12 +689,6 @@
     }
 }
 
-__global__ __launch_bounds__(256) void add_lf_k(float* __restrict__ bpw, const float* __restrict__ lf)
-{
-    int r = blockIdx.x, c = threadIdx.x;
-    bpw[(int64_t)r * 256 + c] += lf[(r >> 7) * 256 + c];
-}
-
 __global__ __launch_bounds__(512) void boxpe_k(
     const float* __restrict__ boxes, const float* __restrict__ sizes, float* __restrict__ boxpe)
 {
@@ -446,48 +711,8 @@
     boxpe[(int64_t)row * 512 + i] = (j & 1) ? cosf(arg) : sinf(arg);
 }
 
-__global__ __launch_bounds__(256) void f36_k(
-    const float* __restrict__ boxes, const float* __restrict__ sizes,
-    unsigned short* __restrict__ f36, int chunk0, int cnt)
-{
-    int li = blockIdx.x * 256 + threadIdx.x;
-    if (li >= cnt) return;
-    int gp = chunk0 + li;
-    int b = gp / P, p = gp - b * P;
-    int xi, yi; pair_xy(p, xi, yi);
-    const float* b1 = boxes + ((int64_t)b * N + xi) * 4;
-    const float* b2 = boxes + ((int64_t)b * N + yi) * 4;
-    float h = sizes[b * 2 + 0], w = sizes[b * 2 + 1];
-    float c1x = (b1[0] + b1[2]) * 0.5f, c1y = (b1[1] + b1[3]) * 0.5f;
-    float c2x = (b2[0] + b2[2]) * 0.5f, c2y = (b2[1] + b2[3]) * 0.5f;
-    float w1 = b1[2] - b1[0], h1 = b1[3] - b1[1];
-    float w2 = b2[2] - b2[0], h2 = b2[3] - b2[1];
-    float a1 = w1 * h1, a2 = w2 * h2;
-    float dx = fabsf(c2x - c1x) / (w1 + 1e-6f);
-    float dy = fabsf(c2y - c1y) / (h1 + 1e-6f);
-    float ix = fmaxf(fminf(b1[2], b2[2]) - fmaxf(b1[0], b2[0]), 0.f);
-    float iy = fmaxf(fminf(b1[3], b2[3]) - fmaxf(b1[1], b2[1]), 0.f);
-    float inter = ix * iy;
-    float iou = inter / (a1 + a2 - inter + 1e-6f);
-    float f[18];
-    f[0] = c1x / w;  f[1] = c1y / h;  f[2] = c2x / w;  f[3] = c2y / h;
-    f[4] = w1 / w;   f[5] = h1 / h;   f[6] = w2 / w;   f[7] = h2 / h;
-    f[8] = a1 / (h * w); f[9] = a2 / (h * w); f[10] = a2 / (a1 + 1e-6f);
-    f[11] = w1 / (h1 + 1e-6f); f[12] = w2 / (h2 + 1e-6f); f[13] = iou;
-    f[14] = (c2x > c1x) ? dx : 0.f;  f[15] = (c2x < c1x) ? dx : 0.f;
-    f[16] = (c2y > c1y) ? dy : 0.f;  f[17] = (c2y < c1y) ? dy : 0.f;
-    unsigned short* o = f36 + (int64_t)li * 64;
-#pragma unroll
-    for (int i = 0; i < 18; ++i) {
-        o[i]      = f2bf(f[i]);
-        o[18 + i] = f2bf(logf(f[i] + 1e-6f));
-    }
-#pragma unroll
-    for (int i = 36; i < 64; ++i) o[i] = 0;
-}
-
 __global__ __launch_bounds__(128) void enc_attn_k(
-    const float* __restrict__ qk, const float* __restrict__ v, float* __restrict__ outp)
+    const float* __restrict__ qkv, float* __restrict__ outp)
 {
     int b = blockIdx.x >> 3, hd = blockIdx.x & 7;
     __shared__ float kl[128][32];
@@ -495,12 +720,13 @@
     int tid = threadIdx.x;
     for (int i = tid; i < 128 * 32; i += 128) {
         int s = i >> 5, j = i & 31;
-        kl[s][j] = qk[((int64_t)(b * 128 + s)) * 512 + 256 + hd * 32 + j];
-        vl[s][j] = v[((int64_t)(b * 128 + s)) * 256 + hd * 32 + j];
+        const float* rp = qkv + ((int64_t)(b * 128 + s)) * 768 + hd * 32 + j;
+        kl[s][j] = rp[256];
+        vl[s][j] = rp[512];
     }
     __syncthreads();
     int t = tid;
-    const float* qp = qk + ((int64_t)(b * 128 + t)) * 512 + hd * 32;
+    const float* qp = qkv + ((int64_t)(b * 128 + t)) * 768 + hd * 32;
     float qr[32];
 #pragma unroll
     for (int j = 0; j < 32; ++j) qr[j] = qp[j] * QSCALE;
@@ -653,14 +879,15 @@
 
     float* posx  = arena;
     float* boxpe = posx  + 524288;
-    float* e_qk  = boxpe + 1048576;
-    float* e_v   = e_qk  + 1048576;
-    float* e_t   = e_v   + 524288;
+    float* pqk0  = boxpe + 1048576;
+    float* pqk1  = pqk0  + 1048576;
+    float* e_qkv = pqk1  + 1048576;
+    float* e_t   = e_qkv + 1572864;
     float* e_ff  = e_t   + 524288;
     float* pctx  = e_ff  + 2097152;
     float* lm    = pctx  + 262144;
 
-    int64_t rc = ((arena_f * 2) / 1088) & ~127LL;
+    int64_t rc = ((arena_f * 2) / 1152) & ~127LL;
     if (rc > BP) rc = BP;
     if (rc < 128) rc = 128;
 
@@ -701,62 +928,58 @@
     line_mean_k<<<8192, 256, 0, stream>>>(line, lm);
     line_proj_k<<<dim3(8, B), 256, 0, stream>>>(lm, lw, lb, lf);
     boxpe_k<<<(int)BN, 512, 0, stream>>>(boxes, sizes, boxpe);
-    bgemm(stream, boxpe, nullptr, 512, wt + WT_EPE, 512, enc_pe_b, posx, 256, (int)BN, 256, 512, false, false);
-    bgemm(stream, boxpe, nullptr, 512, wt + WT_BW,  512, bb,       bpw_, 256, (int)BN, 256, 512, false, false);
-    bgemm(stream, pose,  nullptr, 768, wt + WT_PW,  768, pb,       pctx, 256, B*MPOSE, 256, 768, false, false);
+    bgemm(stream, boxpe, nullptr, 512, wt + WT_EPE, 512, enc_pe_b, nullptr, 0, nullptr, posx, 256, (int)BN, 256, 512, false);
+    bgemm(stream, boxpe, nullptr, 512, wt + WT_BW,  512, bb,       nullptr, 0, lf,      bpw_, 256, (int)BN, 256, 512, false);
+    bgemm(stream, pose,  nullptr, 768, wt + WT_PW,  768, pb,       nullptr, 0, nullptr, pctx, 256, B*MPOSE, 256, 768, false);
     for (int l = 0; l < 2; ++l)
         bgemm(stream, pctx, nullptr, 256, wt + WT_DKV + l*131072, 256, dec_kv_b + (int64_t)l*512,
-              kv0 + (int64_t)l*524288, 512, B*MPOSE, 512, 256, false, false);
-
-    hipMemcpyAsync(x_, embeds, BN * 256 * sizeof(float), hipMemcpyDeviceToDevice, stream);
+              nullptr, 0, nullptr, kv0 + (int64_t)l*524288, 512, B*MPOSE, 512, 256, false);
+    bgemm(stream, posx, nullptr, 256, wt + WT_QKV,          256, nullptr, nullptr, 0, nullptr, pqk0, 512, (int)BN, 512, 256, false);
+    bgemm(stream, posx, nullptr, 256, wt + WT_QKV + 196608, 256, nullptr, nullptr, 0, nullptr, pqk1, 512, (int)BN, 512, 256, false);
+
     for (int i = 0; i < 2; ++i) {
+        const float* xin = (i == 0) ? embeds : x_;
+        const float* pqk = (i == 0) ? pqk0 : pqk1;
         const unsigned short* Wq = wt + WT_QKV + (int64_t)i * 196608;
-        const float* bqkv = enc_qkv_b + (int64_t)i * 768;
-        bgemm(stream, x_, posx, 256, Wq, 256, bqkv, e_qk, 512, (int)BN, 512, 256, false, false);
-        bgemm(stream, x_, nullptr, 256, Wq + 131072, 256, bqkv + 512, e_v, 256, (int)BN, 256, 256, false, false);
-        enc_attn_k<<<B * 8, 128, 0, stream>>>(e_qk, e_v, e_t);
-        bgemm(stream, e_t, nullptr, 256, wt + WT_EOUT + (int64_t)i*65536, 256, enc_out_b + i * 256,
-              e_v, 256, (int)BN, 256, 256, false, false);
-        ln_k<<<(int)(BN / 4), 256, 0, stream>>>(x_, x_, e_v, enc_ln1_g + i * 256, enc_ln1_b + i * 256, (int)BN);
-        bgemm(stream, x_, nullptr, 256, wt + WT_EFF1 + (int64_t)i*262144, 256, enc_ff1_b + i * 1024,
-              e_ff, 1024, (int)BN, 1024, 256, true, false);
-        bgemm(stream, e_ff, nullptr, 1024, wt + WT_EFF2 + (int64_t)i*262144, 1024, enc_ff2_b + i * 256,
-              e_t, 256, (int)BN, 256, 1024, false, false);
-        ln_k<<<(int)(BN / 4), 256, 0, stream>>>(x_, x_, e_t, enc_ln2_g + i * 256, enc_ln2_b + i * 256, (int)BN);
-    }
-
-    add_lf_k<<<(int)BN, 256, 0, stream>>>(bpw_, lf);
+        bgemm(stream, xin, nullptr, 256, Wq, 256, enc_qkv_b + (int64_t)i*768, pqk, 512, nullptr,
+              e_qkv, 768, (int)BN, 768, 256, false);
+        enc_attn_k<<<B * 8, 128, 0, stream>>>(e_qkv, e_t);
+        tgemm_k<<<(int)(BN / 64), 256, 0, stream>>>(e_t, 256, wt + WT_EOUT + (int64_t)i*65536, 256,
+            enc_out_b + i*256, xin, enc_ln1_g + i*256, enc_ln1_b + i*256, x_, 8);
+        bgemm(stream, x_, nullptr, 256, wt + WT_EFF1 + (int64_t)i*262144, 256, enc_ff1_b + i*1024,
+              nullptr, 0, nullptr, e_ff, 1024, (int)BN, 1024, 256, true);
+        tgemm_k<<<(int)(BN / 64), 256, 0, stream>>>(e_ff, 1024, wt + WT_EFF2 + (int64_t)i*262144, 1024,
+            enc_ff2_b + i*256, x_, enc_ln2_g + i*256, enc_ln2_b + i*256, x_, 32);
+    }
+
     for (int l = 0; l < 2; ++l) {
-        bgemm(stream, x_, bpw_, 256, wt + WT_DQ + (int64_t)l*65536, 256, dec_q_b + l * 256,
-              e_v, 256, (int)BN, 256, 256, false, false);
-        dec_attn_k<<<dim3((int)(BN / 256), 8), 256, 0, stream>>>(e_v, kv0 + (int64_t)l*524288, e_t, (int)BN, N);
-        bgemm(stream, e_t, nullptr, 256, wt + WT_DOUT + (int64_t)l*65536, 256, dec_out_b + l * 256,
-              e_v, 256, (int)BN, 256, 256, false, false);
-        ln_k<<<(int)(BN / 4), 256, 0, stream>>>(x_, x_, e_v, dec_ln1_g + l * 256, dec_ln1_b + l * 256, (int)BN);
-        bgemm(stream, x_, nullptr, 256, wt + WT_DFF1 + (int64_t)l*262144, 256, dec_ff1_b + l * 1024,
-              e_ff, 1024, (int)BN, 1024, 256, true, false);
-        bgemm(stream, e_ff, nullptr, 1024, wt + WT_DFF2 + (int64_t)l*262144, 1024, dec_ff2_b + l * 256,
-              e_t, 256, (int)BN, 256, 1024, false, false);
-        ln_k<<<(int)(BN / 4), 256, 0, stream>>>(x_, x_, e_t, dec_ln2_g + l * 256, dec_ln2_b + l * 256, (int)BN);
+        bgemm(stream, x_, bpw_, 256, wt + WT_DQ + (int64_t)l*65536, 256, dec_q_b + l*256,
+              nullptr, 0, nullptr, e_t, 256, (int)BN, 256, 256, false);
+        dec_attn_k<<<dim3((int)(BN / 256), 8), 256, 0, stream>>>(e_t, kv0 + (int64_t)l*524288, e_qkv, (int)BN, N);
+        tgemm_k<<<(int)(BN / 64), 256, 0, stream>>>(e_qkv, 256, wt + WT_DOUT + (int64_t)l*65536, 256,
+            dec_out_b + l*256, x_, dec_ln1_g + l*256, dec_ln1_b + l*256, x_, 8);
+        bgemm(stream, x_, nullptr, 256, wt + WT_DFF1 + (int64_t)l*262144, 256, dec_ff1_b + l*1024,
+              nullptr, 0, nullptr, e_ff, 1024, (int)BN, 1024, 256, true);
+        tgemm_k<<<(int)(BN / 64), 256, 0, stream>>>(e_ff, 1024, wt + WT_DFF2 + (int64_t)l*262144, 1024,
+            dec_ff2_b + l*256, x_, dec_ln2_g + l*256, dec_ln2_b + l*256, x_, 32);
     }
     float* UV = kv0;
-    bgemm(stream, x_, nullptr, 256, wt + WT_FC1, 256, nullptr, UV, 512, (int)BN, 512, 256, false, false);
+    bgemm(stream, x_, nullptr, 256, wt + WT_FC1, 256, nullptr, nullptr, 0, nullptr, UV, 512, (int)BN, 512, 256, false);
 
     for (int64_t c0 = 0; c0 < BP; c0 += rc) {
         int rows = (int)((BP - c0 < rc) ? (BP - c0) : rc);
-        unsigned short* t1  = (unsigned short*)arena;
-        unsigned short* t3  = t1  + (int64_t)rc * 64;
-        unsigned short* tsp = t3  + (int64_t)rc * 256;
-        unsigned short* zb  = tsp + (int64_t)rc * 256;
-
-        f36_k<<<(rows + 255) / 256, 256, 0, stream>>>(boxes, sizes, t1, (int)c0, rows);
-        fgemm_k<false,true,true><<<rows / 128, 256, 0, stream>>>(
-            t1, 64, wt + WT_SW1, 64, sb1, wt + WT_SW2, 128, sb2, t3, 256, 2, 1);
-        fgemm_k<false,false,true><<<rows / 128, 256, 0, stream>>>(
-            t3, 256, wt + WT_SW3, 256, sb3, wt + WT_FC2, 256, fc2_b, tsp, 256, 8, 2);
-        lnh_k<<<rows / 4, 256, 0, stream>>>(zb + 256, 512, tsp, 256, mln2_g, mln2_b, rows);
+        unsigned short* t3 = (unsigned short*)arena;
+        unsigned short* zb = t3 + (int64_t)rc * 256;
+        unsigned short* z2 = zb + (int64_t)rc * 512;
+
+        spa_k<<<rows / 128, 256, 0, stream>>>(boxes, sizes,
+            wt + WT_SW1, sb1, wt + WT_SW2, sb2, t3, (int)c0);
+        sw3fc2ln_k<<<rows / 128, 256, 0, stream>>>(t3,
+            wt + WT_SW3, sb3, wt + WT_FC2, fc2_b, mln2_g, mln2_b, zb + 256, 512);
         pairln_k<<<rows / 4, 256, 0, stream>>>(UV, fc1_b, mln1_g, mln1_b, zb, 512, (int)c0, rows);
-        fgemm_k<true,true,false><<<rows / 128, 256, 0, stream>>>(
-            zb, 512, wt + WT_M1, 512, m1_b, wt + WT_M2, 384, m2_b, out + c0 * 256, 256, 16, 3);
-    }
-}
+        hgemm_k<true,true,true><<<dim3(3, rows / 128), 256, 0, stream>>>(
+            zb, 512, wt + WT_M1, 512, m1_b, z2, 384, 16);
+        hgemm_k<true,false,false><<<dim3(2, rows / 128), 256, 0, stream>>>(
+            z2, 384, wt + WT_M2, 384, m2_b, out + c0 * 256, 256, 12);
+    }
+}
```
